# Performance work log

Hardware: AMD Instinct MI355X
Metric: run time of the kernel (lower is better)

## Reference

```python
import jax, jax.numpy as jnp
import numpy as np

B, N, DIN, DH = 16, 512, 128, 256
NEG = -9.0e15  # matches -9000000000000000.0 in torch source


def _xavier(key, fan_in, fan_out):
    lim = float(np.sqrt(6.0 / (fan_in + fan_out)))
    return jax.random.uniform(key, (fan_in, fan_out), jnp.float32, -lim, lim)


def _l2n(x, eps=1e-12):
    # torch F.normalize: x / max(||x||, eps)
    return x / jnp.maximum(jnp.linalg.norm(x, axis=-1, keepdims=True), eps)


def _prelu(x, a):
    return jnp.where(x >= 0, x, a * x)


def setup_inputs() -> dict:
    key = jax.random.key(0)
    ks = jax.random.split(key, 12)
    seq = jax.random.normal(ks[0], (B, N, DIN), jnp.float32)
    # sparse-ish nonnegative adjacency with self loops, row-normalized
    u = jax.random.uniform(ks[1], (B, N, N), jnp.float32)
    a = jnp.where(u < 0.1, u, 0.0) + jnp.eye(N, dtype=jnp.float32)[None]
    adj = a / a.sum(-1, keepdims=True)
    # dense diffusion matrix, row-normalized
    d = jax.random.uniform(ks[2], (B, N, N), jnp.float32)
    diff = d / d.sum(-1, keepdims=True)
    # dropout keep-mask for F.dropout(p=0.1, training=True)
    keep = jax.random.bernoulli(ks[3], 0.9, (B, N, N)).astype(jnp.float32)
    drop_mask = keep / 0.9
    return {
        "seq": seq, "adj": adj, "diff": diff, "drop_mask": drop_mask,
        "fc1_w": _xavier(ks[4], DIN, DH),
        "q_w": _xavier(ks[5], DH, DH),
        "k_w": _xavier(ks[6], DH, DH),
        "v_w1": _xavier(ks[7], DH, DH),
        "v_w2": _xavier(ks[8], DH, DH),
        "fc2_w": _xavier(ks[9], DIN, DH),
        "bias1": jnp.zeros((DH,), jnp.float32),
        "bias2": jnp.zeros((DH,), jnp.float32),
        "prelu1_a": jnp.float32(0.25),
        "prelu2_a": jnp.float32(0.25),
        "v_prelu_a": jnp.float32(0.25),
    }


def reference(seq, adj, diff, drop_mask, fc1_w, q_w, k_w, v_w1, v_w2,
              fc2_w, bias1, bias2, prelu1_a, prelu2_a, v_prelu_a):
    # ---- GCN1 (attention branch) ----
    fts = seq @ fc1_w                                   # [B,N,H]
    out = jnp.einsum('bmn,bnh->bmh', adj, fts)          # adj aggregation
    q = _l2n(out @ q_w)
    k = _l2n(out @ k_w)
    scores = jax.lax.stop_gradient(jnp.einsum('bmd,bnd->bmn', q, k))  # .detach()
    div_loss = jnp.mean(jnp.sum((q - k) ** 2, axis=-1))
    att = jnp.where(adj > 0, scores, NEG)
    att = jax.nn.softmax(att, axis=-1) * drop_mask      # dropout(p=0.1)
    agg = jnp.einsum('bmn,bnh->bmh', att, out)
    v = _prelu(agg @ v_w1, v_prelu_a) @ v_w2 + bias1
    h1 = _prelu(v, prelu1_a)
    # ---- GCN2 (plain branch) ----
    h2 = _prelu(jnp.einsum('bmn,bnh->bmh', diff, seq @ fc2_w) + bias2, prelu2_a)
    # ---- Readout ----
    c1 = jnp.mean(h1, axis=1)                           # [B,H]
    c2 = jnp.mean(h2, axis=1)
    # ---- DIS ----
    n1 = _l2n(h1).reshape(B * N, DH)
    n2 = _l2n(h2).reshape(B * N, DH)
    node_logits = n1 @ n2.T                             # [B*N, B*N]
    graph_logits = _l2n(c1) @ _l2n(c2).T                # [B, B]
    return node_logits, graph_logits, div_loss
```

## Files before the change

kernel.cpp:

```cpp
#include <hip/hip_runtime.h>
#include <hip/hip_bf16.h>


using bf16x8 = __attribute__((ext_vector_type(8))) short;
using f32x4  = __attribute__((ext_vector_type(4))) float;

__device__ __forceinline__ unsigned short f2b(float f) {
    union { float f; unsigned int u; } x; x.f = f;
    unsigned int r = x.u + 0x7FFFu + ((x.u >> 16) & 1u);
    return (unsigned short)(r >> 16);
}
__device__ __forceinline__ void gload_lds16(const void* g, void* l) {
    __builtin_amdgcn_global_load_lds(
        (const __attribute__((address_space(1))) void*)g,
        (__attribute__((address_space(3))) void*)l, 16, 0, 0);
}

__global__ __launch_bounds__(256) void conv3(const float* __restrict__ seq,
                                             const float* __restrict__ adj,
                                             const float* __restrict__ diff,
                                             unsigned short* __restrict__ seq_bf,
                                             unsigned short* __restrict__ adj_bf,
                                             unsigned short* __restrict__ diff_bf) {
    long i = (long)blockIdx.x * 256 + threadIdx.x;
    const float* src; unsigned short* dst; long off;
    if (i < 262144)       { src = seq;  dst = seq_bf;  off = i; }
    else if (i < 1310720) { src = adj;  dst = adj_bf;  off = i - 262144; }
    else                  { src = diff; dst = diff_bf; off = i - 1310720; }
    float4 v = reinterpret_cast<const float4*>(src)[off];
    ushort4 o; o.x = f2b(v.x); o.y = f2b(v.y); o.z = f2b(v.z); o.w = f2b(v.w);
    reinterpret_cast<ushort4*>(dst)[off] = o;
}

__global__ void wtrans6(const float* __restrict__ fc1, const float* __restrict__ fc2,
                        const float* __restrict__ qw,  const float* __restrict__ kw,
                        const float* __restrict__ v1,  const float* __restrict__ v2,
                        unsigned short* fc1T, unsigned short* fc2T,
                        unsigned short* qwT,  unsigned short* kwT,
                        unsigned short* v1T,  unsigned short* v2T) {
    __shared__ float t[32][33];
    const int z = blockIdx.z;
    const float* in; unsigned short* op; int R;
    const int C = 256;
    if      (z == 0) { in = fc1; op = fc1T; R = 128; }
    else if (z == 1) { in = fc2; op = fc2T; R = 128; }
    else if (z == 2) { in = qw;  op = qwT;  R = 256; }
    else if (z == 3) { in = kw;  op = kwT;  R = 256; }
    else if (z == 4) { in = v1;  op = v1T;  R = 256; }
    else             { in = v2;  op = v2T;  R = 256; }
    int c0 = blockIdx.x * 32, r0 = blockIdx.y * 32;
    if (r0 >= R) return;
    int x = threadIdx.x, y = threadIdx.y;
    for (int i = 0; i < 32; i += 8) t[y + i][x] = in[(long)(r0 + y + i) * C + c0 + x];
    __syncthreads();
    for (int i = 0; i < 32; i += 8)
        op[(long)(c0 + y + i) * R + r0 + x] = f2b(t[x][y + i]);
}

#define BN 128
#define BK 64

template<int TBM, int EPI, bool WF, bool WB, bool WT, bool SWZ>
__global__ __launch_bounds__(256) void gemm_nt(
    const unsigned short* __restrict__ A, const unsigned short* __restrict__ Bt,
    float* __restrict__ Cf, unsigned short* __restrict__ Cb, unsigned short* __restrict__ Ct,
    int M, int Nn, int K, int lda, int ldb, int ldc, int ldt,
    long sA, long sB, long sC, long sT,
    const float* __restrict__ bias, const float* __restrict__ alpha_ptr)
{
    constexpr int MI = TBM / 32;
    __shared__ unsigned short As[TBM][BK];
    __shared__ unsigned short Bs[BN][BK];
    const int b = blockIdx.z;
    A  += (long)b * sA;
    Bt += (long)b * sB;
    const long cbase = (long)b * sC;
    const long tbase = (long)b * sT;

    int tx, ty;
    if (SWZ) {
        int bid = blockIdx.y * gridDim.x + blockIdx.x;
        int nwg = gridDim.x * gridDim.y;
        int cpx = nwg >> 3;
        int s = (bid & 7) * cpx + (bid >> 3);
        tx = s % gridDim.x; ty = s / gridDim.x;
    } else { tx = blockIdx.x; ty = blockIdx.y; }
    const int tile_m = ty * TBM;
    const int tile_n = tx * BN;

    const int tid  = threadIdx.x;
    const int lane = tid & 63;
    const int wave = tid >> 6;
    const int wm = (wave >> 1) * (TBM / 2);
    const int wn = (wave & 1) << 6;
    const int lrow = lane >> 3;
    const int lcol = (lane & 7) << 3;

    f32x4 acc[MI][4] = {};

    for (int k0 = 0; k0 < K; k0 += BK) {
        #pragma unroll
        for (int i = 0; i < TBM / 32; ++i) {
            const int rb = (i * 4 + wave) * 8;
            gload_lds16(A + (long)(tile_m + rb + lrow) * lda + k0 + lcol, &As[rb][0]);
        }
        #pragma unroll
        for (int i = 0; i < 4; ++i) {
            const int rb = (i * 4 + wave) * 8;
            gload_lds16(Bt + (long)(tile_n + rb + lrow) * ldb + k0 + lcol, &Bs[rb][0]);
        }
        __syncthreads();
        #pragma unroll
        for (int ks = 0; ks < 2; ++ks) {
            const int kk = ks * 32 + ((lane >> 4) << 3);
            bf16x8 af[MI], bq[4];
            #pragma unroll
            for (int mi = 0; mi < MI; ++mi)
                af[mi] = *reinterpret_cast<const bf16x8*>(&As[wm + (lane & 15) + mi * 16][kk]);
            #pragma unroll
            for (int ni = 0; ni < 4; ++ni)
                bq[ni] = *reinterpret_cast<const bf16x8*>(&Bs[wn + (lane & 15) + ni * 16][kk]);
            #pragma unroll
            for (int mi = 0; mi < MI; ++mi)
                #pragma unroll
                for (int ni = 0; ni < 4; ++ni)
                    acc[mi][ni] = __builtin_amdgcn_mfma_f32_16x16x32_bf16(
                        af[mi], bq[ni], acc[mi][ni], 0, 0, 0);
        }
        __syncthreads();
    }

    const float alpha = (EPI & 1) ? alpha_ptr[0] : 0.f;
    const int c0 = lane & 15;
    const int r0 = (lane >> 4) << 2;
    #pragma unroll
    for (int ni = 0; ni < 4; ++ni) {
        const int col = tile_n + wn + ni * 16 + c0;
        const float bv = (EPI & 2) ? bias[col] : 0.f;
        #pragma unroll
        for (int mi = 0; mi < MI; ++mi) {
            const int row0 = tile_m + wm + mi * 16 + r0;
            float v[4];
            #pragma unroll
            for (int j = 0; j < 4; ++j) {
                float x = acc[mi][ni][j] + bv;
                if (EPI & 1) x = (x >= 0.f) ? x : alpha * x;
                v[j] = x;
            }
            if (WF) {
                #pragma unroll
                for (int j = 0; j < 4; ++j)
                    Cf[cbase + (long)(row0 + j) * ldc + col] = v[j];
            }
            if (WB) {
                #pragma unroll
                for (int j = 0; j < 4; ++j)
                    Cb[cbase + (long)(row0 + j) * ldc + col] = f2b(v[j]);
            }
            if (WT) {
                ushort4 o; o.x = f2b(v[0]); o.y = f2b(v[1]); o.z = f2b(v[2]); o.w = f2b(v[3]);
                *reinterpret_cast<ushort4*>(&Ct[tbase + (long)col * ldt + row0]) = o;
            }
        }
    }
}

__global__ __launch_bounds__(256) void gemm_norm(
    const unsigned short* __restrict__ A, const unsigned short* __restrict__ Bt,
    unsigned short* __restrict__ n_out, float* __restrict__ psum,
    const float* __restrict__ bias, const float* __restrict__ alpha_ptr,
    int K, int lda, int ldb, long sA, long sB)
{
    __shared__ unsigned short As[32][BK];
    __shared__ unsigned short Bs[256][BK];
    __shared__ float rowred[32][4];
    A  += (long)blockIdx.z * sA;
    Bt += (long)blockIdx.z * sB;
    const int p = blockIdx.z * gridDim.y + blockIdx.y;
    const int arow0 = blockIdx.y * 32;
    const long grow0 = (long)p * 32;

    const int tid  = threadIdx.x;
    const int lane = tid & 63;
    const int wave = tid >> 6;
    const int wn = wave << 6;
    const int lrow = lane >> 3;
    const int lcol = (lane & 7) << 3;

    f32x4 acc[2][4] = {};

    for (int k0 = 0; k0 < K; k0 += BK) {
        {
            const int rb = wave * 8;
            gload_lds16(A + (long)(arow0 + rb + lrow) * lda + k0 + lcol, &As[rb][0]);
        }
        #pragma unroll
        for (int i = 0; i < 8; ++i) {
            const int rb = (i * 4 + wave) * 8;
            gload_lds16(Bt + (long)(rb + lrow) * ldb + k0 + lcol, &Bs[rb][0]);
        }
        __syncthreads();
        #pragma unroll
        for (int ks = 0; ks < 2; ++ks) {
            const int kk = ks * 32 + ((lane >> 4) << 3);
            bf16x8 af[2], bq[4];
            #pragma unroll
            for (int mi = 0; mi < 2; ++mi)
                af[mi] = *reinterpret_cast<const bf16x8*>(&As[(lane & 15) + mi * 16][kk]);
            #pragma unroll
            for (int ni = 0; ni < 4; ++ni)
                bq[ni] = *reinterpret_cast<const bf16x8*>(&Bs[wn + (lane & 15) + ni * 16][kk]);
            #pragma unroll
            for (int mi = 0; mi < 2; ++mi)
                #pragma unroll
                for (int ni = 0; ni < 4; ++ni)
                    acc[mi][ni] = __builtin_amdgcn_mfma_f32_16x16x32_bf16(
                        af[mi], bq[ni], acc[mi][ni], 0, 0, 0);
        }
        __syncthreads();
    }

    const float alpha = alpha_ptr[0];
    const int c0 = lane & 15;
    const int r0 = (lane >> 4) << 2;
    float rs[2][4] = {};
    #pragma unroll
    for (int ni = 0; ni < 4; ++ni) {
        const float bv = bias[wn + ni * 16 + c0];
        #pragma unroll
        for (int mi = 0; mi < 2; ++mi)
            #pragma unroll
            for (int j = 0; j < 4; ++j) {
                float x = acc[mi][ni][j] + bv;
                x = (x >= 0.f) ? x : alpha * x;
                acc[mi][ni][j] = x;
                rs[mi][j] += x * x;
            }
    }
    #pragma unroll
    for (int o = 1; o <= 8; o <<= 1)
        #pragma unroll
        for (int mi = 0; mi < 2; ++mi)
            #pragma unroll
            for (int j = 0; j < 4; ++j) rs[mi][j] += __shfl_xor(rs[mi][j], o);
    if ((lane & 15) == 0) {
        #pragma unroll
        for (int mi = 0; mi < 2; ++mi)
            #pragma unroll
            for (int j = 0; j < 4; ++j) rowred[mi * 16 + r0 + j][wave] = rs[mi][j];
    }
    __syncthreads();
    float inv[2][4];
    #pragma unroll
    for (int mi = 0; mi < 2; ++mi)
        #pragma unroll
        for (int j = 0; j < 4; ++j) {
            const int r = mi * 16 + r0 + j;
            float s = rowred[r][0] + rowred[r][1] + rowred[r][2] + rowred[r][3];
            inv[mi][j] = 1.f / fmaxf(sqrtf(s), 1e-12f);
        }
    float cs[4];
    #pragma unroll
    for (int ni = 0; ni < 4; ++ni) {
        float s = 0.f;
        #pragma unroll
        for (int mi = 0; mi < 2; ++mi)
            #pragma unroll
            for (int j = 0; j < 4; ++j) s += acc[mi][ni][j];
        s += __shfl_xor(s, 16);
        s += __shfl_xor(s, 32);
        cs[ni] = s;
    }
    if (lane < 16) {
        #pragma unroll
        for (int ni = 0; ni < 4; ++ni)
            psum[(long)p * 256 + wn + ni * 16 + lane] = cs[ni];
    }
    #pragma unroll
    for (int ni = 0; ni < 4; ++ni)
        #pragma unroll
        for (int mi = 0; mi < 2; ++mi)
            #pragma unroll
            for (int j = 0; j < 4; ++j)
                n_out[(grow0 + mi * 16 + r0 + j) * 256 + wn + ni * 16 + c0] =
                    f2b(acc[mi][ni][j] * inv[mi][j]);
}

__global__ __launch_bounds__(256) void qk_proj(
    const unsigned short* __restrict__ outb,
    const unsigned short* __restrict__ qkT,
    unsigned short* __restrict__ q_bf,
    unsigned short* __restrict__ k_bf)
{
    __shared__ unsigned short As[32 * 64];
    __shared__ unsigned short Bs[512 * 64];
    __shared__ float sred[32][4];
    const long m0 = (long)blockIdx.x * 32;
    const int tid = threadIdx.x, lane = tid & 63, wave = tid >> 6;
    const int lrow = lane >> 3, lcol = (lane & 7) << 3;
    const int hi = lane >> 4, c0 = lane & 15, r0 = hi << 2;
    const int wn = wave << 7;

    f32x4 acc[2][8] = {};
    for (int k0 = 0; k0 < 256; k0 += 64) {
        gload_lds16(outb + (m0 + wave * 8 + lrow) * 256 + k0 + lcol, &As[wave * 8 * 64]);
        #pragma unroll
        for (int i = 0; i < 16; ++i) {
            const int rb = (i * 4 + wave) * 8;
            gload_lds16(qkT + (long)(rb + lrow) * 256 + k0 + lcol, &Bs[rb * 64]);
        }
        __syncthreads();
        #pragma unroll
        for (int ks = 0; ks < 2; ++ks) {
            const int kk = ks * 32 + (hi << 3);
            bf16x8 af[2], bq[8];
            #pragma unroll
            for (int mi = 0; mi < 2; ++mi)
                af[mi] = *reinterpret_cast<const bf16x8*>(&As[(mi * 16 + c0) * 64 + kk]);
            #pragma unroll
            for (int ni = 0; ni < 8; ++ni)
                bq[ni] = *reinterpret_cast<const bf16x8*>(&Bs[(wn + ni * 16 + c0) * 64 + kk]);
            #pragma unroll
            for (int mi = 0; mi < 2; ++mi)
                #pragma unroll
                for (int ni = 0; ni < 8; ++ni)
                    acc[mi][ni] = __builtin_amdgcn_mfma_f32_16x16x32_bf16(
                        af[mi], bq[ni], acc[mi][ni], 0, 0, 0);
        }
        __syncthreads();
    }
    float rs[2][4] = {};
    #pragma unroll
    for (int mi = 0; mi < 2; ++mi)
        #pragma unroll
        for (int ni = 0; ni < 8; ++ni)
            #pragma unroll
            for (int j = 0; j < 4; ++j) { float x = acc[mi][ni][j]; rs[mi][j] += x * x; }
    #pragma unroll
    for (int o = 1; o <= 8; o <<= 1)
        #pragma unroll
        for (int mi = 0; mi < 2; ++mi)
            #pragma unroll
            for (int j = 0; j < 4; ++j) rs[mi][j] += __shfl_xor(rs[mi][j], o);
    if (c0 == 0) {
        #pragma unroll
        for (int mi = 0; mi < 2; ++mi)
            #pragma unroll
            for (int j = 0; j < 4; ++j) sred[mi * 16 + r0 + j][wave] = rs[mi][j];
    }
    __syncthreads();
    float inv[2][4];
    #pragma unroll
    for (int mi = 0; mi < 2; ++mi)
        #pragma unroll
        for (int j = 0; j < 4; ++j) {
            const int r = mi * 16 + r0 + j;
            float sq = sred[r][0] + sred[r][1];
            float sk = sred[r][2] + sred[r][3];
            inv[mi][j] = 1.f / fmaxf(sqrtf(wave < 2 ? sq : sk), 1e-12f);
        }
    #pragma unroll
    for (int mi = 0; mi < 2; ++mi)
        #pragma unroll
        for (int ni = 0; ni < 8; ++ni)
            #pragma unroll
            for (int j = 0; j < 4; ++j) {
                const long rowg = m0 + mi * 16 + r0 + j;
                const int col = wn + ni * 16 + c0;
                unsigned short v = f2b(acc[mi][ni][j] * inv[mi][j]);
                if (wave < 2) q_bf[rowg * 256 + col] = v;
                else          k_bf[rowg * 256 + col - 256] = v;
            }
}

__global__ __launch_bounds__(256) void att_fused(
    const unsigned short* __restrict__ q_bf,
    const unsigned short* __restrict__ k_bf,
    const unsigned short* __restrict__ adj_bf,
    const float* __restrict__ drop,
    const unsigned short* __restrict__ outT,
    unsigned short* __restrict__ agg_bf,
    float* __restrict__ rowpart)
{
    __shared__ unsigned char smem[69632];
    unsigned short* As  = (unsigned short*)smem;
    unsigned short* Bs  = (unsigned short*)(smem + 4096);
    unsigned short* Pls = (unsigned short*)smem;
    unsigned short* Bs2 = (unsigned short*)(smem + 34816);
    __shared__ float redm[32][4], reds[32][4];

    const int b  = blockIdx.y;
    const int m0 = blockIdx.x << 5;
    const unsigned short* qp = q_bf + (long)b * 131072 + (long)m0 * 256;
    const unsigned short* kp = k_bf + (long)b * 131072;
    const unsigned short* ot = outT + (long)b * 131072;
    const unsigned short* ap = adj_bf + ((long)b * 512 + m0) * 512;
    const float*          dp = drop   + ((long)b * 512 + m0) * 512;

    const int tid = threadIdx.x, lane = tid & 63, wave = tid >> 6;
    const int lrow = lane >> 3, lcol = (lane & 7) << 3;
    const int hi = lane >> 4, c0 = lane & 15, r0 = hi << 2;
    const int wn = wave << 7;

    f32x4 acc[2][8] = {};
    for (int k0 = 0; k0 < 256; k0 += 64) {
        gload_lds16(qp + (long)(wave * 8 + lrow) * 256 + k0 + lcol, &As[wave * 8 * 64]);
        #pragma unroll
        for (int i = 0; i < 16; ++i) {
            const int rb = (i * 4 + wave) * 8;
            gload_lds16(kp + (long)(rb + lrow) * 256 + k0 + lcol, &Bs[rb * 64]);
        }
        __syncthreads();
        #pragma unroll
        for (int ks = 0; ks < 2; ++ks) {
            const int kk = ks * 32 + (hi << 3);
            bf16x8 af[2], bq[8];
            #pragma unroll
            for (int mi = 0; mi < 2; ++mi)
                af[mi] = *reinterpret_cast<const bf16x8*>(&As[(mi * 16 + c0) * 64 + kk]);
            #pragma unroll
            for (int ni = 0; ni < 8; ++ni)
                bq[ni] = *reinterpret_cast<const bf16x8*>(&Bs[(wn + ni * 16 + c0) * 64 + kk]);
            #pragma unroll
            for (int mi = 0; mi < 2; ++mi)
                #pragma unroll
                for (int ni = 0; ni < 8; ++ni)
                    acc[mi][ni] = __builtin_amdgcn_mfma_f32_16x16x32_bf16(
                        af[mi], bq[ni], acc[mi][ni], 0, 0, 0);
        }
        __syncthreads();
    }

    float rmax[2][4];
    #pragma unroll
    for (int mi = 0; mi < 2; ++mi)
        #pragma unroll
        for (int j = 0; j < 4; ++j) rmax[mi][j] = -3.0e38f;
    #pragma unroll
    for (int mi = 0; mi < 2; ++mi)
        #pragma unroll
        for (int ni = 0; ni < 8; ++ni)
            #pragma unroll
            for (int j = 0; j < 4; ++j) {
                const int rowl = mi * 16 + r0 + j;
                const int col  = wn + ni * 16 + c0;
                float s = acc[mi][ni][j];
                if (col == m0 + rowl)
                    rowpart[(long)b * 512 + m0 + rowl] = 2.f - 2.f * s;
                bool m = ap[(long)rowl * 512 + col] != 0;
                s = m ? s : -3.0e38f;
                acc[mi][ni][j] = s;
                rmax[mi][j] = fmaxf(rmax[mi][j], s);
            }
    #pragma unroll
    for (int o = 1; o <= 8; o <<= 1)
        #pragma unroll
        for (int mi = 0; mi < 2; ++mi)
            #pragma unroll
            for (int j = 0; j < 4; ++j) rmax[mi][j] = fmaxf(rmax[mi][j], __shfl_xor(rmax[mi][j], o));
    if (c0 == 0) {
        #pragma unroll
        for (int mi = 0; mi < 2; ++mi)
            #pragma unroll
            for (int j = 0; j < 4; ++j) redm[mi * 16 + r0 + j][wave] = rmax[mi][j];
    }
    __syncthreads();
    float mx[2][4], rsum[2][4];
    #pragma unroll
    for (int mi = 0; mi < 2; ++mi)
        #pragma unroll
        for (int j = 0; j < 4; ++j) {
            const int r = mi * 16 + r0 + j;
            mx[mi][j] = fmaxf(fmaxf(redm[r][0], redm[r][1]), fmaxf(redm[r][2], redm[r][3]));
            rsum[mi][j] = 0.f;
        }
    #pragma unroll
    for (int mi = 0; mi < 2; ++mi)
        #pragma unroll
        for (int ni = 0; ni < 8; ++ni)
            #pragma unroll
            for (int j = 0; j < 4; ++j) {
                float e = __expf(acc[mi][ni][j] - mx[mi][j]);
                acc[mi][ni][j] = e;
                rsum[mi][j] += e;
            }
    #pragma unroll
    for (int o = 1; o <= 8; o <<= 1)
        #pragma unroll
        for (int mi = 0; mi < 2; ++mi)
            #pragma unroll
            for (int j = 0; j < 4; ++j) rsum[mi][j] += __shfl_xor(rsum[mi][j], o);
    if (c0 == 0) {
        #pragma unroll
        for (int mi = 0; mi < 2; ++mi)
            #pragma unroll
            for (int j = 0; j < 4; ++j) reds[mi * 16 + r0 + j][wave] = rsum[mi][j];
    }
    __syncthreads();
    float inv[2][4];
    #pragma unroll
    for (int mi = 0; mi < 2; ++mi)
        #pragma unroll
        for (int j = 0; j < 4; ++j) {
            const int r = mi * 16 + r0 + j;
            inv[mi][j] = 1.f / (reds[r][0] + reds[r][1] + reds[r][2] + reds[r][3]);
        }
    #pragma unroll
    for (int mi = 0; mi < 2; ++mi)
        #pragma unroll
        for (int ni = 0; ni < 8; ++ni)
            #pragma unroll
            for (int j = 0; j < 4; ++j) {
                const int rowl = mi * 16 + r0 + j;
                const int col  = wn + ni * 16 + c0;
                float p = acc[mi][ni][j] * inv[mi][j] * dp[(long)rowl * 512 + col];
                Pls[rowl * 520 + col] = f2b(p);
            }
    __syncthreads();

    f32x4 acc2[2][4] = {};
    for (int k0 = 0; k0 < 512; k0 += 64) {
        #pragma unroll
        for (int i = 0; i < 8; ++i) {
            const int rb = (i * 4 + wave) * 8;
            gload_lds16(ot + (long)(rb + lrow) * 512 + k0 + lcol, &Bs2[rb * 64]);
        }
        __syncthreads();
        #pragma unroll
        for (int ks = 0; ks < 2; ++ks) {
            const int kk = ks * 32 + (hi << 3);
            bf16x8 af[2], bq[4];
            #pragma unroll
            for (int mi = 0; mi < 2; ++mi)
                af[mi] = *reinterpret_cast<const bf16x8*>(&Pls[(mi * 16 + c0) * 520 + k0 + kk]);
            #pragma unroll
            for (int ni = 0; ni < 4; ++ni)
                bq[ni] = *reinterpret_cast<const bf16x8*>(&Bs2[((wave << 6) + ni * 16 + c0) * 64 + kk]);
            #pragma unroll
            for (int mi = 0; mi < 2; ++mi)
                #pragma unroll
                for (int ni = 0; ni < 4; ++ni)
                    acc2[mi][ni] = __builtin_amdgcn_mfma_f32_16x16x32_bf16(
                        af[mi], bq[ni], acc2[mi][ni], 0, 0, 0);
        }
        __syncthreads();
    }
    #pragma unroll
    for (int mi = 0; mi < 2; ++mi)
        #pragma unroll
        for (int ni = 0; ni < 4; ++ni)
            #pragma unroll
            for (int j = 0; j < 4; ++j) {
                const int rowl = mi * 16 + r0 + j;
                const int col  = (wave << 6) + ni * 16 + c0;
                agg_bf[((long)b * 512 + m0 + rowl) * 256 + col] = f2b(acc2[mi][ni][j]);
            }
}

__global__ __launch_bounds__(256) void mlp_norm(
    const unsigned short* __restrict__ agg,
    const unsigned short* __restrict__ w1T,
    const unsigned short* __restrict__ w2T,
    const float* __restrict__ bias,
    const float* __restrict__ av, const float* __restrict__ a1,
    unsigned short* __restrict__ n_out,
    float* __restrict__ psum)
{
    __shared__ unsigned char smem[49664];
    unsigned short* As  = (unsigned short*)smem;
    unsigned short* Bs  = (unsigned short*)(smem + 4096);
    unsigned short* T   = (unsigned short*)smem;
    unsigned short* Bs2 = (unsigned short*)(smem + 16896);
    __shared__ float rowred[32][4];

    const int p = blockIdx.x;
    const long row0 = (long)p * 32;
    const int tid = threadIdx.x, lane = tid & 63, wave = tid >> 6;
    const int lrow = lane >> 3, lcol = (lane & 7) << 3;
    const int hi = lane >> 4, c0 = lane & 15, r0 = hi << 2;
    const int wn = wave << 6;

    f32x4 acc[2][4] = {};
    for (int k0 = 0; k0 < 256; k0 += 64) {
        gload_lds16(agg + (row0 + wave * 8 + lrow) * 256 + k0 + lcol, &As[wave * 8 * 64]);
        #pragma unroll
        for (int i = 0; i < 8; ++i) {
            const int rb = (i * 4 + wave) * 8;
            gload_lds16(w1T + (long)(rb + lrow) * 256 + k0 + lcol, &Bs[rb * 64]);
        }
        __syncthreads();
        #pragma unroll
        for (int ks = 0; ks < 2; ++ks) {
            const int kk = ks * 32 + (hi << 3);
            bf16x8 af[2], bq[4];
            #pragma unroll
            for (int mi = 0; mi < 2; ++mi)
                af[mi] = *reinterpret_cast<const bf16x8*>(&As[(mi * 16 + c0) * 64 + kk]);
            #pragma unroll
            for (int ni = 0; ni < 4; ++ni)
                bq[ni] = *reinterpret_cast<const bf16x8*>(&Bs[(wn + ni * 16 + c0) * 64 + kk]);
            #pragma unroll
            for (int mi = 0; mi < 2; ++mi)
                #pragma unroll
                for (int ni = 0; ni < 4; ++ni)
                    acc[mi][ni] = __builtin_amdgcn_mfma_f32_16x16x32_bf16(
                        af[mi], bq[ni], acc[mi][ni], 0, 0, 0);
        }
        __syncthreads();
    }
    const float alphav = av[0];
    #pragma unroll
    for (int mi = 0; mi < 2; ++mi)
        #pragma unroll
        for (int ni = 0; ni < 4; ++ni)
            #pragma unroll
            for (int j = 0; j < 4; ++j) {
                const int rowl = mi * 16 + r0 + j;
                const int col  = wn + ni * 16 + c0;
                float x = acc[mi][ni][j];
                x = (x >= 0.f) ? x : alphav * x;
                T[rowl * 264 + col] = f2b(x);
            }
    __syncthreads();

    f32x4 acc2[2][4] = {};
    for (int k0 = 0; k0 < 256; k0 += 64) {
        #pragma unroll
        for (int i = 0; i < 8; ++i) {
            const int rb = (i * 4 + wave) * 8;
            gload_lds16(w2T + (long)(rb + lrow) * 256 + k0 + lcol, &Bs2[rb * 64]);
        }
        __syncthreads();
        #pragma unroll
        for (int ks = 0; ks < 2; ++ks) {
            const int kk = ks * 32 + (hi << 3);
            bf16x8 af[2], bq[4];
            #pragma unroll
            for (int mi = 0; mi < 2; ++mi)
                af[mi] = *reinterpret_cast<const bf16x8*>(&T[(mi * 16 + c0) * 264 + k0 + kk]);
            #pragma unroll
            for (int ni = 0; ni < 4; ++ni)
                bq[ni] = *reinterpret_cast<const bf16x8*>(&Bs2[(wn + ni * 16 + c0) * 64 + kk]);
            #pragma unroll
            for (int mi = 0; mi < 2; ++mi)
                #pragma unroll
                for (int ni = 0; ni < 4; ++ni)
                    acc2[mi][ni] = __builtin_amdgcn_mfma_f32_16x16x32_bf16(
                        af[mi], bq[ni], acc2[mi][ni], 0, 0, 0);
        }
        __syncthreads();
    }
    const float alpha1 = a1[0];
    float rs[2][4] = {};
    #pragma unroll
    for (int ni = 0; ni < 4; ++ni) {
        const float bv = bias[wn + ni * 16 + c0];
        #pragma unroll
        for (int mi = 0; mi < 2; ++mi)
            #pragma unroll
            for (int j = 0; j < 4; ++j) {
                float x = acc2[mi][ni][j] + bv;
                x = (x >= 0.f) ? x : alpha1 * x;
                acc2[mi][ni][j] = x;
                rs[mi][j] += x * x;
            }
    }
    #pragma unroll
    for (int o = 1; o <= 8; o <<= 1)
        #pragma unroll
        for (int mi = 0; mi < 2; ++mi)
            #pragma unroll
            for (int j = 0; j < 4; ++j) rs[mi][j] += __shfl_xor(rs[mi][j], o);
    if (c0 == 0) {
        #pragma unroll
        for (int mi = 0; mi < 2; ++mi)
            #pragma unroll
            for (int j = 0; j < 4; ++j) rowred[mi * 16 + r0 + j][wave] = rs[mi][j];
    }
    __syncthreads();
    float inv[2][4];
    #pragma unroll
    for (int mi = 0; mi < 2; ++mi)
        #pragma unroll
        for (int j = 0; j < 4; ++j) {
            const int r = mi * 16 + r0 + j;
            float s = rowred[r][0] + rowred[r][1] + rowred[r][2] + rowred[r][3];
            inv[mi][j] = 1.f / fmaxf(sqrtf(s), 1e-12f);
        }
    float cs[4];
    #pragma unroll
    for (int ni = 0; ni < 4; ++ni) {
        float s = 0.f;
        #pragma unroll
        for (int mi = 0; mi < 2; ++mi)
            #pragma unroll
            for (int j = 0; j < 4; ++j) s += acc2[mi][ni][j];
        s += __shfl_xor(s, 16);
        s += __shfl_xor(s, 32);
        cs[ni] = s;
    }
    if (lane < 16) {
        #pragma unroll
        for (int ni = 0; ni < 4; ++ni)
            psum[(long)p * 256 + wn + ni * 16 + lane] = cs[ni];
    }
    #pragma unroll
    for (int mi = 0; mi < 2; ++mi)
        #pragma unroll
        for (int ni = 0; ni < 4; ++ni)
            #pragma unroll
            for (int j = 0; j < 4; ++j)
                n_out[(row0 + mi * 16 + r0 + j) * 256 + wn + ni * 16 + c0] =
                    f2b(acc2[mi][ni][j] * inv[mi][j]);
}

__global__ __launch_bounds__(256) void creduce(const float* __restrict__ psum1,
                                               const float* __restrict__ psum2,
                                               float* __restrict__ c1n,
                                               float* __restrict__ c2n) {
    const int which = blockIdx.x & 1, g = blockIdx.x >> 1;
    const float* ps = which ? psum2 : psum1;
    float* cn = which ? c2n : c1n;
    const int t = threadIdx.x;
    float s = 0.f;
    #pragma unroll
    for (int c = 0; c < 16; ++c) s += ps[(long)(g * 16 + c) * 256 + t];
    s *= (1.f / 512.f);
    float ss = s * s;
    #pragma unroll
    for (int o = 32; o; o >>= 1) ss += __shfl_xor(ss, o);
    __shared__ float red[4];
    if ((t & 63) == 0) red[t >> 6] = ss;
    __syncthreads();
    float tot = red[0] + red[1] + red[2] + red[3];
    cn[g * 256 + t] = s / fmaxf(sqrtf(tot), 1e-12f);
}

__global__ __launch_bounds__(256) void graphf3(const float* __restrict__ c1n,
                                               const float* __restrict__ c2n,
                                               const float* __restrict__ rowpart,
                                               float* __restrict__ out_g,
                                               float* __restrict__ out_div) {
    const int t = threadIdx.x, ii = t >> 4, jj = t & 15;
    float s = 0.f;
    for (int h = 0; h < 256; ++h) s += c1n[ii * 256 + h] * c2n[jj * 256 + h];
    out_g[ii * 16 + jj] = s;
    float ds = 0.f;
    for (int i = t; i < 8192; i += 256) ds += rowpart[i];
    #pragma unroll
    for (int o = 32; o; o >>= 1) ds += __shfl_xor(ds, o);
    __shared__ float red[4];
    if ((t & 63) == 0) red[t >> 6] = ds;
    __syncthreads();
    if (t == 0) out_div[0] = (red[0] + red[1] + red[2] + red[3]) * (1.f / 8192.f);
}

static constexpr long OFF_SEQ_BF  = 0;
static constexpr long OFF_FC1T    = 2097152;
static constexpr long OFF_QWT     = 2228224;
static constexpr long OFF_VW1T    = 2490368;
static constexpr long OFF_VW2T    = 2621440;
static constexpr long OFF_ROWPART = 2752512;
static constexpr long OFF_C1N     = 2785280;
static constexpr long OFF_C2N     = 2801664;
static constexpr long OFF_ADJ     = 3145728;
static constexpr long OFF_DIFF    = 11534336;
static constexpr long OFF_FTST    = 19922944;
static constexpr long OFF_OUTT    = 28311552;
static constexpr long OFF_OUTBF   = 32505856;
static constexpr long OFF_QBF     = 36700160;
static constexpr long OFF_KBF     = 40894464;
static constexpr long OFF_AGG     = 45088768;
static constexpr long OFF_PSUM    = 49283072;
static constexpr long OFF_N1      = 49807360;
static constexpr long OFF_N2      = 54001664;

extern "C" void kernel_launch(void* const* d_in, const int* in_sizes, int n_in,
                              void* d_out, int out_size, void* d_ws, size_t ws_size,
                              hipStream_t stream) {
    const float* seq      = (const float*)d_in[0];
    const float* adj      = (const float*)d_in[1];
    const float* diff     = (const float*)d_in[2];
    const float* drop     = (const float*)d_in[3];
    const float* fc1_w    = (const float*)d_in[4];
    const float* q_w      = (const float*)d_in[5];
    const float* k_w      = (const float*)d_in[6];
    const float* v_w1     = (const float*)d_in[7];
    const float* v_w2     = (const float*)d_in[8];
    const float* fc2_w    = (const float*)d_in[9];
    const float* bias1    = (const float*)d_in[10];
    const float* bias2    = (const float*)d_in[11];
    const float* prelu1_a = (const float*)d_in[12];
    const float* prelu2_a = (const float*)d_in[13];
    const float* v_prelu  = (const float*)d_in[14];
    float* out = (float*)d_out;

    char* ws = (char*)d_ws;
    unsigned short* seq_bf  = (unsigned short*)(ws + OFF_SEQ_BF);
    unsigned short* fc1T    = (unsigned short*)(ws + OFF_FC1T);
    unsigned short* fc2T    = (unsigned short*)(ws + OFF_FC1T + 65536);
    unsigned short* qwT     = (unsigned short*)(ws + OFF_QWT);
    unsigned short* kwT     = (unsigned short*)(ws + OFF_QWT + 131072);
    unsigned short* vw1T    = (unsigned short*)(ws + OFF_VW1T);
    unsigned short* vw2T    = (unsigned short*)(ws + OFF_VW2T);
    float*          rowpart = (float*)(ws + OFF_ROWPART);
    float*          c1n     = (float*)(ws + OFF_C1N);
    float*          c2n     = (float*)(ws + OFF_C2N);
    unsigned short* adj_bf  = (unsigned short*)(ws + OFF_ADJ);
    unsigned short* diff_bf = (unsigned short*)(ws + OFF_DIFF);
    unsigned short* ftsT    = (unsigned short*)(ws + OFF_FTST);
    unsigned short* fts2T   = (unsigned short*)(ws + OFF_FTST + 4194304);
    unsigned short* outT    = (unsigned short*)(ws + OFF_OUTT);
    unsigned short* out_bf  = (unsigned short*)(ws + OFF_OUTBF);
    unsigned short* q_bf    = (unsigned short*)(ws + OFF_QBF);
    unsigned short* k_bf    = (unsigned short*)(ws + OFF_KBF);
    unsigned short* agg_bf  = (unsigned short*)(ws + OFF_AGG);
    float*          psum1   = (float*)(ws + OFF_PSUM);
    float*          psum2   = (float*)(ws + OFF_PSUM + 262144);
    unsigned short* n1_bf   = (unsigned short*)(ws + OFF_N1);
    unsigned short* n2_bf   = (unsigned short*)(ws + OFF_N2);

    conv3<<<9216, 256, 0, stream>>>(seq, adj, diff, seq_bf, adj_bf, diff_bf);
    wtrans6<<<dim3(8, 8, 6), dim3(32, 8), 0, stream>>>(
        fc1_w, fc2_w, q_w, k_w, v_w1, v_w2, fc1T, fc2T, qwT, kwT, vw1T, vw2T);

    gemm_nt<64, 0, false, true, false, false><<<dim3(64, 4, 2), 256, 0, stream>>>(
        fc1T, seq_bf, nullptr, ftsT, nullptr,
        256, 8192, 128, 128, 128, 8192, 0, 32768, 0, 2097152, 0, nullptr, nullptr);

    gemm_nt<64, 0, false, true, true, false><<<dim3(2, 8, 16), 256, 0, stream>>>(
        adj_bf, ftsT, nullptr, out_bf, outT,
        512, 256, 512, 512, 8192, 256, 512, 262144, 512, 131072, 131072, nullptr, nullptr);

    gemm_norm<<<dim3(1, 16, 16), 256, 0, stream>>>(
        diff_bf, fts2T, n2_bf, psum2, bias2, prelu2_a, 512, 512, 8192, 262144, 512);

    qk_proj<<<256, 256, 0, stream>>>(out_bf, qwT, q_bf, k_bf);

    att_fused<<<dim3(16, 16), 256, 0, stream>>>(
        q_bf, k_bf, adj_bf, drop, outT, agg_bf, rowpart);

    mlp_norm<<<256, 256, 0, stream>>>(
        agg_bf, vw1T, vw2T, bias1, v_prelu, prelu1_a, n1_bf, psum1);

    creduce<<<32, 256, 0, stream>>>(psum1, psum2, c1n, c2n);
    graphf3<<<1, 256, 0, stream>>>(c1n, c2n, rowpart, out + 67108864, out + 67109120);

    gemm_nt<128, 0, true, false, false, true><<<dim3(64, 64, 1), 256, 0, stream>>>(
        n1_bf, n2_bf, out, nullptr, nullptr,
        8192, 8192, 256, 256, 256, 8192, 0, 0, 0, 0, 0, nullptr, nullptr);

    (void)in_sizes; (void)n_in; (void)out_size; (void)ws_size;
}
```

Before: 209.3 us.

## Fuse GCN1 aggregation with QK projection and attention with MLP kernels

Merges the fp32-to-bf16 conversion and weight-transpose kernels into one prep launch. Fuses the adj aggregation GEMM with the q/k projection and normalisation, keeping the aggregated rows in LDS instead of round-tripping out_bf. Fuses the attention kernel with the two-layer MLP and norm so the agg intermediate never goes to global memory. The large node-logit GEMM output switches to nontemporal stores. Together these cut launches and intermediate traffic, at the cost of more LDS per block and lower occupancy in the fused kernels.

New measurement: 212.5 us. About the same (+1.5%).

```diff
diff --git a/kernel.cpp b/kernel.cpp
--- a/kernel.cpp
+++ b/kernel.cpp
@@ -16,42 +16,43 @@
         (__attribute__((address_space(3))) void*)l, 16, 0, 0);
 }
 
-__global__ __launch_bounds__(256) void conv3(const float* __restrict__ seq,
-                                             const float* __restrict__ adj,
-                                             const float* __restrict__ diff,
-                                             unsigned short* __restrict__ seq_bf,
-                                             unsigned short* __restrict__ adj_bf,
-                                             unsigned short* __restrict__ diff_bf) {
-    long i = (long)blockIdx.x * 256 + threadIdx.x;
-    const float* src; unsigned short* dst; long off;
-    if (i < 262144)       { src = seq;  dst = seq_bf;  off = i; }
-    else if (i < 1310720) { src = adj;  dst = adj_bf;  off = i - 262144; }
-    else                  { src = diff; dst = diff_bf; off = i - 1310720; }
-    float4 v = reinterpret_cast<const float4*>(src)[off];
-    ushort4 o; o.x = f2b(v.x); o.y = f2b(v.y); o.z = f2b(v.z); o.w = f2b(v.w);
-    reinterpret_cast<ushort4*>(dst)[off] = o;
-}
-
-__global__ void wtrans6(const float* __restrict__ fc1, const float* __restrict__ fc2,
-                        const float* __restrict__ qw,  const float* __restrict__ kw,
-                        const float* __restrict__ v1,  const float* __restrict__ v2,
-                        unsigned short* fc1T, unsigned short* fc2T,
-                        unsigned short* qwT,  unsigned short* kwT,
-                        unsigned short* v1T,  unsigned short* v2T) {
+__global__ __launch_bounds__(256) void prep(
+    const float* __restrict__ seq, const float* __restrict__ adj,
+    const float* __restrict__ diff,
+    const float* __restrict__ fc1, const float* __restrict__ fc2,
+    const float* __restrict__ qw,  const float* __restrict__ kw,
+    const float* __restrict__ v1,  const float* __restrict__ v2,
+    unsigned short* __restrict__ seq_bf, unsigned short* __restrict__ adj_bf,
+    unsigned short* __restrict__ diff_bf,
+    unsigned short* fc1T, unsigned short* fc2T, unsigned short* qwT,
+    unsigned short* kwT,  unsigned short* v1T,  unsigned short* v2T)
+{
     __shared__ float t[32][33];
-    const int z = blockIdx.z;
+    const int bid = blockIdx.x, tid = threadIdx.x;
+    if (bid < 9216) {
+        long i = (long)bid * 256 + tid;
+        const float* src; unsigned short* dst; long off;
+        if (i < 262144)       { src = seq;  dst = seq_bf;  off = i; }
+        else if (i < 1310720) { src = adj;  dst = adj_bf;  off = i - 262144; }
+        else                  { src = diff; dst = diff_bf; off = i - 1310720; }
+        float4 v = reinterpret_cast<const float4*>(src)[off];
+        ushort4 o; o.x = f2b(v.x); o.y = f2b(v.y); o.z = f2b(v.z); o.w = f2b(v.w);
+        reinterpret_cast<ushort4*>(dst)[off] = o;
+        return;
+    }
+    const int r = bid - 9216;
+    const int z = r >> 6;
     const float* in; unsigned short* op; int R;
-    const int C = 256;
     if      (z == 0) { in = fc1; op = fc1T; R = 128; }
     else if (z == 1) { in = fc2; op = fc2T; R = 128; }
     else if (z == 2) { in = qw;  op = qwT;  R = 256; }
     else if (z == 3) { in = kw;  op = kwT;  R = 256; }
     else if (z == 4) { in = v1;  op = v1T;  R = 256; }
     else             { in = v2;  op = v2T;  R = 256; }
-    int c0 = blockIdx.x * 32, r0 = blockIdx.y * 32;
+    const int c0 = (r & 7) * 32, r0 = ((r >> 3) & 7) * 32;
     if (r0 >= R) return;
-    int x = threadIdx.x, y = threadIdx.y;
-    for (int i = 0; i < 32; i += 8) t[y + i][x] = in[(long)(r0 + y + i) * C + c0 + x];
+    const int x = tid & 31, y = tid >> 5;
+    for (int i = 0; i < 32; i += 8) t[y + i][x] = in[(long)(r0 + y + i) * 256 + c0 + x];
     __syncthreads();
     for (int i = 0; i < 32; i += 8)
         op[(long)(c0 + y + i) * R + r0 + x] = f2b(t[x][y + i]);
@@ -60,13 +61,12 @@
 #define BN 128
 #define BK 64
 
-template<int TBM, int EPI, bool WF, bool WB, bool WT, bool SWZ>
+template<int TBM, bool WF, bool WB, bool SWZ>
 __global__ __launch_bounds__(256) void gemm_nt(
     const unsigned short* __restrict__ A, const unsigned short* __restrict__ Bt,
-    float* __restrict__ Cf, unsigned short* __restrict__ Cb, unsigned short* __restrict__ Ct,
-    int M, int Nn, int K, int lda, int ldb, int ldc, int ldt,
-    long sA, long sB, long sC, long sT,
-    const float* __restrict__ bias, const float* __restrict__ alpha_ptr)
+    float* __restrict__ Cf, unsigned short* __restrict__ Cb,
+    int M, int Nn, int K, int lda, int ldb, int ldc,
+    long sA, long sB, long sC)
 {
     constexpr int MI = TBM / 32;
     __shared__ unsigned short As[TBM][BK];
@@ -75,7 +75,6 @@
     A  += (long)b * sA;
     Bt += (long)b * sB;
     const long cbase = (long)b * sC;
-    const long tbase = (long)b * sT;
 
     int tx, ty;
     if (SWZ) {
@@ -130,39 +129,500 @@
         __syncthreads();
     }
 
-    const float alpha = (EPI & 1) ? alpha_ptr[0] : 0.f;
     const int c0 = lane & 15;
     const int r0 = (lane >> 4) << 2;
     #pragma unroll
     for (int ni = 0; ni < 4; ++ni) {
         const int col = tile_n + wn + ni * 16 + c0;
-        const float bv = (EPI & 2) ? bias[col] : 0.f;
         #pragma unroll
         for (int mi = 0; mi < MI; ++mi) {
             const int row0 = tile_m + wm + mi * 16 + r0;
-            float v[4];
+            if (WF) {
+                #pragma unroll
+                for (int j = 0; j < 4; ++j)
+                    __builtin_nontemporal_store(acc[mi][ni][j],
+                        &Cf[cbase + (long)(row0 + j) * ldc + col]);
+            }
+            if (WB) {
+                #pragma unroll
+                for (int j = 0; j < 4; ++j)
+                    Cb[cbase + (long)(row0 + j) * ldc + col] = f2b(acc[mi][ni][j]);
+            }
+        }
+    }
+}
+
+__global__ __launch_bounds__(256) void gcn1qk(
+    const unsigned short* __restrict__ adj_bf,
+    const unsigned short* __restrict__ ftsT,
+    const unsigned short* __restrict__ qkT,
+    unsigned short* __restrict__ outT,
+    unsigned short* __restrict__ q_bf,
+    unsigned short* __restrict__ k_bf)
+{
+    __shared__ unsigned char smem[86528];
+    unsigned short* Ot  = (unsigned short*)smem;
+    unsigned short* As  = (unsigned short*)(smem + 16896);
+    unsigned short* Bs  = (unsigned short*)(smem + 20992);
+    unsigned short* Bs2 = (unsigned short*)(smem + 20992);
+    __shared__ float sred[32][4];
+
+    const int b  = blockIdx.y;
+    const int m0 = blockIdx.x << 5;
+    const unsigned short* ap = adj_bf + ((long)b * 512 + m0) * 512;
+
+    const int tid = threadIdx.x, lane = tid & 63, wave = tid >> 6;
+    const int lrow = lane >> 3, lcol = (lane & 7) << 3;
+    const int hi = lane >> 4, c0 = lane & 15, r0 = hi << 2;
+
+    {
+        const int wn = wave << 6;
+        f32x4 acc[2][4] = {};
+        for (int k0 = 0; k0 < 512; k0 += 64) {
+            gload_lds16(ap + (long)(wave * 8 + lrow) * 512 + k0 + lcol, &As[wave * 8 * 64]);
+            #pragma unroll
+            for (int i = 0; i < 8; ++i) {
+                const int rb = (i * 4 + wave) * 8;
+                gload_lds16(ftsT + (long)(rb + lrow) * 8192 + b * 512 + k0 + lcol, &Bs[rb * 64]);
+            }
+            __syncthreads();
+            #pragma unroll
+            for (int ks = 0; ks < 2; ++ks) {
+                const int kk = ks * 32 + (hi << 3);
+                bf16x8 af[2], bq[4];
+                #pragma unroll
+                for (int mi = 0; mi < 2; ++mi)
+                    af[mi] = *reinterpret_cast<const bf16x8*>(&As[(mi * 16 + c0) * 64 + kk]);
+                #pragma unroll
+                for (int ni = 0; ni < 4; ++ni)
+                    bq[ni] = *reinterpret_cast<const bf16x8*>(&Bs[(wn + ni * 16 + c0) * 64 + kk]);
+                #pragma unroll
+                for (int mi = 0; mi < 2; ++mi)
+                    #pragma unroll
+                    for (int ni = 0; ni < 4; ++ni)
+                        acc[mi][ni] = __builtin_amdgcn_mfma_f32_16x16x32_bf16(
+                            af[mi], bq[ni], acc[mi][ni], 0, 0, 0);
+            }
+            __syncthreads();
+        }
+        #pragma unroll
+        for (int mi = 0; mi < 2; ++mi)
+            #pragma unroll
+            for (int ni = 0; ni < 4; ++ni) {
+                const int col = wn + ni * 16 + c0;
+                ushort4 o;
+                unsigned short* e = (unsigned short*)&o;
+                #pragma unroll
+                for (int j = 0; j < 4; ++j) {
+                    unsigned short v = f2b(acc[mi][ni][j]);
+                    e[j] = v;
+                    Ot[(mi * 16 + r0 + j) * 264 + col] = v;
+                }
+                *reinterpret_cast<ushort4*>(
+                    &outT[(long)b * 131072 + (long)col * 512 + m0 + mi * 16 + r0]) = o;
+            }
+    }
+    __syncthreads();
+
+    {
+        const int wn = wave << 7;
+        f32x4 acc[2][8] = {};
+        for (int k0 = 0; k0 < 256; k0 += 64) {
+            #pragma unroll
+            for (int i = 0; i < 16; ++i) {
+                const int rb = (i * 4 + wave) * 8;
+                gload_lds16(qkT + (long)(rb + lrow) * 256 + k0 + lcol, &Bs2[rb * 64]);
+            }
+            __syncthreads();
+            #pragma unroll
+            for (int ks = 0; ks < 2; ++ks) {
+                const int kk = ks * 32 + (hi << 3);
+                bf16x8 af[2], bq[8];
+                #pragma unroll
+                for (int mi = 0; mi < 2; ++mi)
+                    af[mi] = *reinterpret_cast<const bf16x8*>(&Ot[(mi * 16 + c0) * 264 + k0 + kk]);
+                #pragma unroll
+                for (int ni = 0; ni < 8; ++ni)
+                    bq[ni] = *reinterpret_cast<const bf16x8*>(&Bs2[(wn + ni * 16 + c0) * 64 + kk]);
+                #pragma unroll
+                for (int mi = 0; mi < 2; ++mi)
+                    #pragma unroll
+                    for (int ni = 0; ni < 8; ++ni)
+                        acc[mi][ni] = __builtin_amdgcn_mfma_f32_16x16x32_bf16(
+                            af[mi], bq[ni], acc[mi][ni], 0, 0, 0);
+            }
+            __syncthreads();
+        }
+        float rs[2][4] = {};
+        #pragma unroll
+        for (int mi = 0; mi < 2; ++mi)
+            #pragma unroll
+            for (int ni = 0; ni < 8; ++ni)
+                #pragma unroll
+                for (int j = 0; j < 4; ++j) { float x = acc[mi][ni][j]; rs[mi][j] += x * x; }
+        #pragma unroll
+        for (int o = 1; o <= 8; o <<= 1)
+            #pragma unroll
+            for (int mi = 0; mi < 2; ++mi)
+                #pragma unroll
+                for (int j = 0; j < 4; ++j) rs[mi][j] += __shfl_xor(rs[mi][j], o);
+        if (c0 == 0) {
+            #pragma unroll
+            for (int mi = 0; mi < 2; ++mi)
+                #pragma unroll
+                for (int j = 0; j < 4; ++j) sred[mi * 16 + r0 + j][wave] = rs[mi][j];
+        }
+        __syncthreads();
+        float inv[2][4];
+        #pragma unroll
+        for (int mi = 0; mi < 2; ++mi)
             #pragma unroll
             for (int j = 0; j < 4; ++j) {
-                float x = acc[mi][ni][j] + bv;
-                if (EPI & 1) x = (x >= 0.f) ? x : alpha * x;
-                v[j] = x;
-            }
-            if (WF) {
+                const int rr = mi * 16 + r0 + j;
+                float sq = sred[rr][0] + sred[rr][1];
+                float sk = sred[rr][2] + sred[rr][3];
+                inv[mi][j] = 1.f / fmaxf(sqrtf(wave < 2 ? sq : sk), 1e-12f);
+            }
+        #pragma unroll
+        for (int mi = 0; mi < 2; ++mi)
+            #pragma unroll
+            for (int ni = 0; ni < 8; ++ni)
+                #pragma unroll
+                for (int j = 0; j < 4; ++j) {
+                    const long rowg = (long)b * 512 + m0 + mi * 16 + r0 + j;
+                    const int col = wn + ni * 16 + c0;
+                    unsigned short v = f2b(acc[mi][ni][j] * inv[mi][j]);
+                    if (wave < 2) q_bf[rowg * 256 + col] = v;
+                    else          k_bf[rowg * 256 + col - 256] = v;
+                }
+    }
+}
+
+__global__ __launch_bounds__(256) void attmlp(
+    const unsigned short* __restrict__ q_bf,
+    const unsigned short* __restrict__ k_bf,
+    const unsigned short* __restrict__ adj_bf,
+    const float* __restrict__ drop,
+    const unsigned short* __restrict__ outT,
+    const unsigned short* __restrict__ w1T,
+    const unsigned short* __restrict__ w2T,
+    const float* __restrict__ bias,
+    const float* __restrict__ av, const float* __restrict__ a1,
+    unsigned short* __restrict__ n_out,
+    float* __restrict__ psum,
+    float* __restrict__ rowpart)
+{
+    __shared__ unsigned char smem[69632];
+    unsigned short* As  = (unsigned short*)smem;
+    unsigned short* Bs  = (unsigned short*)(smem + 4096);
+    unsigned short* Pls = (unsigned short*)smem;
+    unsigned short* Bs2 = (unsigned short*)(smem + 34816);
+    unsigned short* T   = (unsigned short*)smem;
+    unsigned short* Bs3 = (unsigned short*)(smem + 16896);
+    __shared__ float redm[32][4], reds[32][4];
+
+    const int b  = blockIdx.y;
+    const int m0 = blockIdx.x << 5;
+    const unsigned short* qp = q_bf + (long)b * 131072 + (long)m0 * 256;
+    const unsigned short* kp = k_bf + (long)b * 131072;
+    const unsigned short* ot = outT + (long)b * 131072;
+    const unsigned short* ap = adj_bf + ((long)b * 512 + m0) * 512;
+    const float*          dp = drop   + ((long)b * 512 + m0) * 512;
+
+    const int tid = threadIdx.x, lane = tid & 63, wave = tid >> 6;
+    const int lrow = lane >> 3, lcol = (lane & 7) << 3;
+    const int hi = lane >> 4, c0 = lane & 15, r0 = hi << 2;
+
+    {
+        const int wn = wave << 7;
+        f32x4 acc[2][8] = {};
+        for (int k0 = 0; k0 < 256; k0 += 64) {
+            gload_lds16(qp + (long)(wave * 8 + lrow) * 256 + k0 + lcol, &As[wave * 8 * 64]);
+            #pragma unroll
+            for (int i = 0; i < 16; ++i) {
+                const int rb = (i * 4 + wave) * 8;
+                gload_lds16(kp + (long)(rb + lrow) * 256 + k0 + lcol, &Bs[rb * 64]);
+            }
+            __syncthreads();
+            #pragma unroll
+            for (int ks = 0; ks < 2; ++ks) {
+                const int kk = ks * 32 + (hi << 3);
+                bf16x8 af[2], bq[8];
+                #pragma unroll
+                for (int mi = 0; mi < 2; ++mi)
+                    af[mi] = *reinterpret_cast<const bf16x8*>(&As[(mi * 16 + c0) * 64 + kk]);
+                #pragma unroll
+                for (int ni = 0; ni < 8; ++ni)
+                    bq[ni] = *reinterpret_cast<const bf16x8*>(&Bs[(wn + ni * 16 + c0) * 64 + kk]);
+                #pragma unroll
+                for (int mi = 0; mi < 2; ++mi)
+                    #pragma unroll
+                    for (int ni = 0; ni < 8; ++ni)
+                        acc[mi][ni] = __builtin_amdgcn_mfma_f32_16x16x32_bf16(
+                            af[mi], bq[ni], acc[mi][ni], 0, 0, 0);
+            }
+            __syncthreads();
+        }
+
+        float rmax[2][4];
+        #pragma unroll
+        for (int mi = 0; mi < 2; ++mi)
+            #pragma unroll
+            for (int j = 0; j < 4; ++j) rmax[mi][j] = -3.0e38f;
+        #pragma unroll
+        for (int mi = 0; mi < 2; ++mi)
+            #pragma unroll
+            for (int ni = 0; ni < 8; ++ni)
+                #pragma unroll
+                for (int j = 0; j < 4; ++j) {
+                    const int rowl = mi * 16 + r0 + j;
+                    const int col  = wn + ni * 16 + c0;
+                    float s = acc[mi][ni][j];
+                    if (col == m0 + rowl)
+                        rowpart[(long)b * 512 + m0 + rowl] = 2.f - 2.f * s;
+                    bool m = ap[(long)rowl * 512 + col] != 0;
+                    s = m ? s : -3.0e38f;
+                    acc[mi][ni][j] = s;
+                    rmax[mi][j] = fmaxf(rmax[mi][j], s);
+                }
+        #pragma unroll
+        for (int o = 1; o <= 8; o <<= 1)
+            #pragma unroll
+            for (int mi = 0; mi < 2; ++mi)
                 #pragma unroll
                 for (int j = 0; j < 4; ++j)
-                    Cf[cbase + (long)(row0 + j) * ldc + col] = v[j];
-            }
-            if (WB) {
-                #pragma unroll
-                for (int j = 0; j < 4; ++j)
-                    Cb[cbase + (long)(row0 + j) * ldc + col] = f2b(v[j]);
-            }
-            if (WT) {
-                ushort4 o; o.x = f2b(v[0]); o.y = f2b(v[1]); o.z = f2b(v[2]); o.w = f2b(v[3]);
-                *reinterpret_cast<ushort4*>(&Ct[tbase + (long)col * ldt + row0]) = o;
-            }
-        }
-    }
+                    rmax[mi][j] = fmaxf(rmax[mi][j], __shfl_xor(rmax[mi][j], o));
+        if (c0 == 0) {
+            #pragma unroll
+            for (int mi = 0; mi < 2; ++mi)
+                #pragma unroll
+                for (int j = 0; j < 4; ++j) redm[mi * 16 + r0 + j][wave] = rmax[mi][j];
+        }
+        __syncthreads();
+        float mx[2][4], rsum[2][4];
+        #pragma unroll
+        for (int mi = 0; mi < 2; ++mi)
+            #pragma unroll
+            for (int j = 0; j < 4; ++j) {
+                const int rr = mi * 16 + r0 + j;
+                mx[mi][j] = fmaxf(fmaxf(redm[rr][0], redm[rr][1]), fmaxf(redm[rr][2], redm[rr][3]));
+                rsum[mi][j] = 0.f;
+            }
+        #pragma unroll
+        for (int mi = 0; mi < 2; ++mi)
+            #pragma unroll
+            for (int ni = 0; ni < 8; ++ni)
+                #pragma unroll
+                for (int j = 0; j < 4; ++j) {
+                    float e = __expf(acc[mi][ni][j] - mx[mi][j]);
+                    acc[mi][ni][j] = e;
+                    rsum[mi][j] += e;
+                }
+        #pragma unroll
+        for (int o = 1; o <= 8; o <<= 1)
+            #pragma unroll
+            for (int mi = 0; mi < 2; ++mi)
+                #pragma unroll
+                for (int j = 0; j < 4; ++j) rsum[mi][j] += __shfl_xor(rsum[mi][j], o);
+        if (c0 == 0) {
+            #pragma unroll
+            for (int mi = 0; mi < 2; ++mi)
+                #pragma unroll
+                for (int j = 0; j < 4; ++j) reds[mi * 16 + r0 + j][wave] = rsum[mi][j];
+        }
+        __syncthreads();
+        float inv[2][4];
+        #pragma unroll
+        for (int mi = 0; mi < 2; ++mi)
+            #pragma unroll
+            for (int j = 0; j < 4; ++j) {
+                const int rr = mi * 16 + r0 + j;
+                inv[mi][j] = 1.f / (reds[rr][0] + reds[rr][1] + reds[rr][2] + reds[rr][3]);
+            }
+        #pragma unroll
+        for (int mi = 0; mi < 2; ++mi)
+            #pragma unroll
+            for (int ni = 0; ni < 8; ++ni)
+                #pragma unroll
+                for (int j = 0; j < 4; ++j) {
+                    const int rowl = mi * 16 + r0 + j;
+                    const int col  = wn + ni * 16 + c0;
+                    float p = acc[mi][ni][j] * inv[mi][j] * dp[(long)rowl * 512 + col];
+                    Pls[rowl * 520 + col] = f2b(p);
+                }
+    }
+    __syncthreads();
+
+    f32x4 acc2[2][4] = {};
+    {
+        const int wn = wave << 6;
+        for (int k0 = 0; k0 < 512; k0 += 64) {
+            #pragma unroll
+            for (int i = 0; i < 8; ++i) {
+                const int rb = (i * 4 + wave) * 8;
+                gload_lds16(ot + (long)(rb + lrow) * 512 + k0 + lcol, &Bs2[rb * 64]);
+            }
+            __syncthreads();
+            #pragma unroll
+            for (int ks = 0; ks < 2; ++ks) {
+                const int kk = ks * 32 + (hi << 3);
+                bf16x8 af[2], bq[4];
+                #pragma unroll
+                for (int mi = 0; mi < 2; ++mi)
+                    af[mi] = *reinterpret_cast<const bf16x8*>(&Pls[(mi * 16 + c0) * 520 + k0 + kk]);
+                #pragma unroll
+                for (int ni = 0; ni < 4; ++ni)
+                    bq[ni] = *reinterpret_cast<const bf16x8*>(&Bs2[(wn + ni * 16 + c0) * 64 + kk]);
+                #pragma unroll
+                for (int mi = 0; mi < 2; ++mi)
+                    #pragma unroll
+                    for (int ni = 0; ni < 4; ++ni)
+                        acc2[mi][ni] = __builtin_amdgcn_mfma_f32_16x16x32_bf16(
+                            af[mi], bq[ni], acc2[mi][ni], 0, 0, 0);
+            }
+            __syncthreads();
+        }
+    }
+
+    const int wn6 = wave << 6;
+    const float alphav = av[0];
+    #pragma unroll
+    for (int mi = 0; mi < 2; ++mi)
+        #pragma unroll
+        for (int ni = 0; ni < 4; ++ni)
+            #pragma unroll
+            for (int j = 0; j < 4; ++j)
+                T[(mi * 16 + r0 + j) * 264 + wn6 + ni * 16 + c0] = f2b(acc2[mi][ni][j]);
+    f32x4 acct[2][4] = {};
+    for (int k0 = 0; k0 < 256; k0 += 64) {
+        #pragma unroll
+        for (int i = 0; i < 8; ++i) {
+            const int rb = (i * 4 + wave) * 8;
+            gload_lds16(w1T + (long)(rb + lrow) * 256 + k0 + lcol, &Bs3[rb * 64]);
+        }
+        __syncthreads();
+        #pragma unroll
+        for (int ks = 0; ks < 2; ++ks) {
+            const int kk = ks * 32 + (hi << 3);
+            bf16x8 af[2], bq[4];
+            #pragma unroll
+            for (int mi = 0; mi < 2; ++mi)
+                af[mi] = *reinterpret_cast<const bf16x8*>(&T[(mi * 16 + c0) * 264 + k0 + kk]);
+            #pragma unroll
+            for (int ni = 0; ni < 4; ++ni)
+                bq[ni] = *reinterpret_cast<const bf16x8*>(&Bs3[(wn6 + ni * 16 + c0) * 64 + kk]);
+            #pragma unroll
+            for (int mi = 0; mi < 2; ++mi)
+                #pragma unroll
+                for (int ni = 0; ni < 4; ++ni)
+                    acct[mi][ni] = __builtin_amdgcn_mfma_f32_16x16x32_bf16(
+                        af[mi], bq[ni], acct[mi][ni], 0, 0, 0);
+        }
+        __syncthreads();
+    }
+    #pragma unroll
+    for (int mi = 0; mi < 2; ++mi)
+        #pragma unroll
+        for (int ni = 0; ni < 4; ++ni)
+            #pragma unroll
+            for (int j = 0; j < 4; ++j) {
+                float x = acct[mi][ni][j];
+                x = (x >= 0.f) ? x : alphav * x;
+                T[(mi * 16 + r0 + j) * 264 + wn6 + ni * 16 + c0] = f2b(x);
+            }
+
+    f32x4 acc3[2][4] = {};
+    for (int k0 = 0; k0 < 256; k0 += 64) {
+        #pragma unroll
+        for (int i = 0; i < 8; ++i) {
+            const int rb = (i * 4 + wave) * 8;
+            gload_lds16(w2T + (long)(rb + lrow) * 256 + k0 + lcol, &Bs3[rb * 64]);
+        }
+        __syncthreads();
+        #pragma unroll
+        for (int ks = 0; ks < 2; ++ks) {
+            const int kk = ks * 32 + (hi << 3);
+            bf16x8 af[2], bq[4];
+            #pragma unroll
+            for (int mi = 0; mi < 2; ++mi)
+                af[mi] = *reinterpret_cast<const bf16x8*>(&T[(mi * 16 + c0) * 264 + k0 + kk]);
+            #pragma unroll
+            for (int ni = 0; ni < 4; ++ni)
+                bq[ni] = *reinterpret_cast<const bf16x8*>(&Bs3[(wn6 + ni * 16 + c0) * 64 + kk]);
+            #pragma unroll
+            for (int mi = 0; mi < 2; ++mi)
+                #pragma unroll
+                for (int ni = 0; ni < 4; ++ni)
+                    acc3[mi][ni] = __builtin_amdgcn_mfma_f32_16x16x32_bf16(
+                        af[mi], bq[ni], acc3[mi][ni], 0, 0, 0);
+        }
+        __syncthreads();
+    }
+
+    const float alpha1 = a1[0];
+    float rs[2][4] = {};
+    #pragma unroll
+    for (int ni = 0; ni < 4; ++ni) {
+        const float bv = bias[wn6 + ni * 16 + c0];
+        #pragma unroll
+        for (int mi = 0; mi < 2; ++mi)
+            #pragma unroll
+            for (int j = 0; j < 4; ++j) {
+                float x = acc3[mi][ni][j] + bv;
+                x = (x >= 0.f) ? x : alpha1 * x;
+                acc3[mi][ni][j] = x;
+                rs[mi][j] += x * x;
+            }
+    }
+    #pragma unroll
+    for (int o = 1; o <= 8; o <<= 1)
+        #pragma unroll
+        for (int mi = 0; mi < 2; ++mi)
+            #pragma unroll
+            for (int j = 0; j < 4; ++j) rs[mi][j] += __shfl_xor(rs[mi][j], o);
+    if (c0 == 0) {
+        #pragma unroll
+        for (int mi = 0; mi < 2; ++mi)
+            #pragma unroll
+            for (int j = 0; j < 4; ++j) redm[mi * 16 + r0 + j][wave] = rs[mi][j];
+    }
+    __syncthreads();
+    float inv2[2][4];
+    #pragma unroll
+    for (int mi = 0; mi < 2; ++mi)
+        #pragma unroll
+        for (int j = 0; j < 4; ++j) {
+            const int rr = mi * 16 + r0 + j;
+            float s = redm[rr][0] + redm[rr][1] + redm[rr][2] + redm[rr][3];
+            inv2[mi][j] = 1.f / fmaxf(sqrtf(s), 1e-12f);
+        }
+    float cs[4];
+    #pragma unroll
+    for (int ni = 0; ni < 4; ++ni) {
+        float s = 0.f;
+        #pragma unroll
+        for (int mi = 0; mi < 2; ++mi)
+            #pragma unroll
+            for (int j = 0; j < 4; ++j) s += acc3[mi][ni][j];
+        s += __shfl_xor(s, 16);
+        s += __shfl_xor(s, 32);
+        cs[ni] = s;
+    }
+    const int p = b * 16 + blockIdx.x;
+    if (lane < 16) {
+        #pragma unroll
+        for (int ni = 0; ni < 4; ++ni)
+            psum[(long)p * 256 + wn6 + ni * 16 + lane] = cs[ni];
+    }
+    const long row0g = (long)b * 512 + m0;
+    #pragma unroll
+    for (int mi = 0; mi < 2; ++mi)
+        #pragma unroll
+        for (int ni = 0; ni < 4; ++ni)
+            #pragma unroll
+            for (int j = 0; j < 4; ++j)
+                n_out[(row0g + mi * 16 + r0 + j) * 256 + wn6 + ni * 16 + c0] =
+                    f2b(acc3[mi][ni][j] * inv2[mi][j]);
 }
 
 __global__ __launch_bounds__(256) void gemm_norm(
@@ -286,434 +746,6 @@
                     f2b(acc[mi][ni][j] * inv[mi][j]);
 }
 
-__global__ __launch_bounds__(256) void qk_proj(
-    const unsigned short* __restrict__ outb,
-    const unsigned short* __restrict__ qkT,
-    unsigned short* __restrict__ q_bf,
-    unsigned short* __restrict__ k_bf)
-{
-    __shared__ unsigned short As[32 * 64];
-    __shared__ unsigned short Bs[512 * 64];
-    __shared__ float sred[32][4];
-    const long m0 = (long)blockIdx.x * 32;
-    const int tid = threadIdx.x, lane = tid & 63, wave = tid >> 6;
-    const int lrow = lane >> 3, lcol = (lane & 7) << 3;
-    const int hi = lane >> 4, c0 = lane & 15, r0 = hi << 2;
-    const int wn = wave << 7;
-
-    f32x4 acc[2][8] = {};
-    for (int k0 = 0; k0 < 256; k0 += 64) {
-        gload_lds16(outb + (m0 + wave * 8 + lrow) * 256 + k0 + lcol, &As[wave * 8 * 64]);
-        #pragma unroll
-        for (int i = 0; i < 16; ++i) {
-            const int rb = (i * 4 + wave) * 8;
-            gload_lds16(qkT + (long)(rb + lrow) * 256 + k0 + lcol, &Bs[rb * 64]);
-        }
-        __syncthreads();
-        #pragma unroll
-        for (int ks = 0; ks < 2; ++ks) {
-            const int kk = ks * 32 + (hi << 3);
-            bf16x8 af[2], bq[8];
-            #pragma unroll
-            for (int mi = 0; mi < 2; ++mi)
-                af[mi] = *reinterpret_cast<const bf16x8*>(&As[(mi * 16 + c0) * 64 + kk]);
-            #pragma unroll
-            for (int ni = 0; ni < 8; ++ni)
-                bq[ni] = *reinterpret_cast<const bf16x8*>(&Bs[(wn + ni * 16 + c0) * 64 + kk]);
-            #pragma unroll
-            for (int mi = 0; mi < 2; ++mi)
-                #pragma unroll
-                for (int ni = 0; ni < 8; ++ni)
-                    acc[mi][ni] = __builtin_amdgcn_mfma_f32_16x16x32_bf16(
-                        af[mi], bq[ni], acc[mi][ni], 0, 0, 0);
-        }
-        __syncthreads();
-    }
-    float rs[2][4] = {};
-    #pragma unroll
-    for (int mi = 0; mi < 2; ++mi)
-        #pragma unroll
-        for (int ni = 0; ni < 8; ++ni)
-            #pragma unroll
-            for (int j = 0; j < 4; ++j) { float x = acc[mi][ni][j]; rs[mi][j] += x * x; }
-    #pragma unroll
-    for (int o = 1; o <= 8; o <<= 1)
-        #pragma unroll
-        for (int mi = 0; mi < 2; ++mi)
-            #pragma unroll
-            for (int j = 0; j < 4; ++j) rs[mi][j] += __shfl_xor(rs[mi][j], o);
-    if (c0 == 0) {
-        #pragma unroll
-        for (int mi = 0; mi < 2; ++mi)
-            #pragma unroll
-            for (int j = 0; j < 4; ++j) sred[mi * 16 + r0 + j][wave] = rs[mi][j];
-    }
-    __syncthreads();
-    float inv[2][4];
-    #pragma unroll
-    for (int mi = 0; mi < 2; ++mi)
-        #pragma unroll
-        for (int j = 0; j < 4; ++j) {
-            const int r = mi * 16 + r0 + j;
-            float sq = sred[r][0] + sred[r][1];
-            float sk = sred[r][2] + sred[r][3];
-            inv[mi][j] = 1.f / fmaxf(sqrtf(wave < 2 ? sq : sk), 1e-12f);
-        }
-    #pragma unroll
-    for (int mi = 0; mi < 2; ++mi)
-        #pragma unroll
-        for (int ni = 0; ni < 8; ++ni)
-            #pragma unroll
-            for (int j = 0; j < 4; ++j) {
-                const long rowg = m0 + mi * 16 + r0 + j;
-                const int col = wn + ni * 16 + c0;
-                unsigned short v = f2b(acc[mi][ni][j] * inv[mi][j]);
-                if (wave < 2) q_bf[rowg * 256 + col] = v;
-                else          k_bf[rowg * 256 + col - 256] = v;
-            }
-}
-
-__global__ __launch_bounds__(256) void att_fused(
-    const unsigned short* __restrict__ q_bf,
-    const unsigned short* __restrict__ k_bf,
-    const unsigned short* __restrict__ adj_bf,
-    const float* __restrict__ drop,
-    const unsigned short* __restrict__ outT,
-    unsigned short* __restrict__ agg_bf,
-    float* __restrict__ rowpart)
-{
-    __shared__ unsigned char smem[69632];
-    unsigned short* As  = (unsigned short*)smem;
-    unsigned short* Bs  = (unsigned short*)(smem + 4096);
-    unsigned short* Pls = (unsigned short*)smem;
-    unsigned short* Bs2 = (unsigned short*)(smem + 34816);
-    __shared__ float redm[32][4], reds[32][4];
-
-    const int b  = blockIdx.y;
-    const int m0 = blockIdx.x << 5;
-    const unsigned short* qp = q_bf + (long)b * 131072 + (long)m0 * 256;
-    const unsigned short* kp = k_bf + (long)b * 131072;
-    const unsigned short* ot = outT + (long)b * 131072;
-    const unsigned short* ap = adj_bf + ((long)b * 512 + m0) * 512;
-    const float*          dp = drop   + ((long)b * 512 + m0) * 512;
-
-    const int tid = threadIdx.x, lane = tid & 63, wave = tid >> 6;
-    const int lrow = lane >> 3, lcol = (lane & 7) << 3;
-    const int hi = lane >> 4, c0 = lane & 15, r0 = hi << 2;
-    const int wn = wave << 7;
-
-    f32x4 acc[2][8] = {};
-    for (int k0 = 0; k0 < 256; k0 += 64) {
-        gload_lds16(qp + (long)(wave * 8 + lrow) * 256 + k0 + lcol, &As[wave * 8 * 64]);
-        #pragma unroll
-        for (int i = 0; i < 16; ++i) {
-            const int rb = (i * 4 + wave) * 8;
-            gload_lds16(kp + (long)(rb + lrow) * 256 + k0 + lcol, &Bs[rb * 64]);
-        }
-        __syncthreads();
-        #pragma unroll
-        for (int ks = 0; ks < 2; ++ks) {
-            const int kk = ks * 32 + (hi << 3);
-            bf16x8 af[2], bq[8];
-            #pragma unroll
-            for (int mi = 0; mi < 2; ++mi)
-                af[mi] = *reinterpret_cast<const bf16x8*>(&As[(mi * 16 + c0) * 64 + kk]);
-            #pragma unroll
-            for (int ni = 0; ni < 8; ++ni)
-                bq[ni] = *reinterpret_cast<const bf16x8*>(&Bs[(wn + ni * 16 + c0) * 64 + kk]);
-            #pragma unroll
-            for (int mi = 0; mi < 2; ++mi)
-                #pragma unroll
-                for (int ni = 0; ni < 8; ++ni)
-                    acc[mi][ni] = __builtin_amdgcn_mfma_f32_16x16x32_bf16(
-                        af[mi], bq[ni], acc[mi][ni], 0, 0, 0);
-        }
-        __syncthreads();
-    }
-
-    float rmax[2][4];
-    #pragma unroll
-    for (int mi = 0; mi < 2; ++mi)
-        #pragma unroll
-        for (int j = 0; j < 4; ++j) rmax[mi][j] = -3.0e38f;
-    #pragma unroll
-    for (int mi = 0; mi < 2; ++mi)
-        #pragma unroll
-        for (int ni = 0; ni < 8; ++ni)
-            #pragma unroll
-            for (int j = 0; j < 4; ++j) {
-                const int rowl = mi * 16 + r0 + j;
-                const int col  = wn + ni * 16 + c0;
-                float s = acc[mi][ni][j];
-                if (col == m0 + rowl)
-                    rowpart[(long)b * 512 + m0 + rowl] = 2.f - 2.f * s;
-                bool m = ap[(long)rowl * 512 + col] != 0;
-                s = m ? s : -3.0e38f;
-                acc[mi][ni][j] = s;
-                rmax[mi][j] = fmaxf(rmax[mi][j], s);
-            }
-    #pragma unroll
-    for (int o = 1; o <= 8; o <<= 1)
-        #pragma unroll
-        for (int mi = 0; mi < 2; ++mi)
-            #pragma unroll
-            for (int j = 0; j < 4; ++j) rmax[mi][j] = fmaxf(rmax[mi][j], __shfl_xor(rmax[mi][j], o));
-    if (c0 == 0) {
-        #pragma unroll
-        for (int mi = 0; mi < 2; ++mi)
-            #pragma unroll
-            for (int j = 0; j < 4; ++j) redm[mi * 16 + r0 + j][wave] = rmax[mi][j];
-    }
-    __syncthreads();
-    float mx[2][4], rsum[2][4];
-    #pragma unroll
-    for (int mi = 0; mi < 2; ++mi)
-        #pragma unroll
-        for (int j = 0; j < 4; ++j) {
-            const int r = mi * 16 + r0 + j;
-            mx[mi][j] = fmaxf(fmaxf(redm[r][0], redm[r][1]), fmaxf(redm[r][2], redm[r][3]));
-            rsum[mi][j] = 0.f;
-        }
-    #pragma unroll
-    for (int mi = 0; mi < 2; ++mi)
-        #pragma unroll
-        for (int ni = 0; ni < 8; ++ni)
-            #pragma unroll
-            for (int j = 0; j < 4; ++j) {
-                float e = __expf(acc[mi][ni][j] - mx[mi][j]);
-                acc[mi][ni][j] = e;
-                rsum[mi][j] += e;
-            }
-    #pragma unroll
-    for (int o = 1; o <= 8; o <<= 1)
-        #pragma unroll
-        for (int mi = 0; mi < 2; ++mi)
-            #pragma unroll
-            for (int j = 0; j < 4; ++j) rsum[mi][j] += __shfl_xor(rsum[mi][j], o);
-    if (c0 == 0) {
-        #pragma unroll
-        for (int mi = 0; mi < 2; ++mi)
-            #pragma unroll
-            for (int j = 0; j < 4; ++j) reds[mi * 16 + r0 + j][wave] = rsum[mi][j];
-    }
-    __syncthreads();
-    float inv[2][4];
-    #pragma unroll
-    for (int mi = 0; mi < 2; ++mi)
-        #pragma unroll
-        for (int j = 0; j < 4; ++j) {
-            const int r = mi * 16 + r0 + j;
-            inv[mi][j] = 1.f / (reds[r][0] + reds[r][1] + reds[r][2] + reds[r][3]);
-        }
-    #pragma unroll
-    for (int mi = 0; mi < 2; ++mi)
-        #pragma unroll
-        for (int ni = 0; ni < 8; ++ni)
-            #pragma unroll
-            for (int j = 0; j < 4; ++j) {
-                const int rowl = mi * 16 + r0 + j;
-                const int col  = wn + ni * 16 + c0;
-                float p = acc[mi][ni][j] * inv[mi][j] * dp[(long)rowl * 512 + col];
-                Pls[rowl * 520 + col] = f2b(p);
-            }
-    __syncthreads();
-
-    f32x4 acc2[2][4] = {};
-    for (int k0 = 0; k0 < 512; k0 += 64) {
-        #pragma unroll
-        for (int i = 0; i < 8; ++i) {
-            const int rb = (i * 4 + wave) * 8;
-            gload_lds16(ot + (long)(rb + lrow) * 512 + k0 + lcol, &Bs2[rb * 64]);
-        }
-        __syncthreads();
-        #pragma unroll
-        for (int ks = 0; ks < 2; ++ks) {
-            const int kk = ks * 32 + (hi << 3);
-            bf16x8 af[2], bq[4];
-            #pragma unroll
-            for (int mi = 0; mi < 2; ++mi)
-                af[mi] = *reinterpret_cast<const bf16x8*>(&Pls[(mi * 16 + c0) * 520 + k0 + kk]);
-            #pragma unroll
-            for (int ni = 0; ni < 4; ++ni)
-                bq[ni] = *reinterpret_cast<const bf16x8*>(&Bs2[((wave << 6) + ni * 16 + c0) * 64 + kk]);
-            #pragma unroll
-            for (int mi = 0; mi < 2; ++mi)
-                #pragma unroll
-                for (int ni = 0; ni < 4; ++ni)
-                    acc2[mi][ni] = __builtin_amdgcn_mfma_f32_16x16x32_bf16(
-                        af[mi], bq[ni], acc2[mi][ni], 0, 0, 0);
-        }
-        __syncthreads();
-    }
-    #pragma unroll
-    for (int mi = 0; mi < 2; ++mi)
-        #pragma unroll
-        for (int ni = 0; ni < 4; ++ni)
-            #pragma unroll
-            for (int j = 0; j < 4; ++j) {
-                const int rowl = mi * 16 + r0 + j;
-                const int col  = (wave << 6) + ni * 16 + c0;
-                agg_bf[((long)b * 512 + m0 + rowl) * 256 + col] = f2b(acc2[mi][ni][j]);
-            }
-}
-
-__global__ __launch_bounds__(256) void mlp_norm(
-    const unsigned short* __restrict__ agg,
-    const unsigned short* __restrict__ w1T,
-    const unsigned short* __restrict__ w2T,
-    const float* __restrict__ bias,
-    const float* __restrict__ av, const float* __restrict__ a1,
-    unsigned short* __restrict__ n_out,
-    float* __restrict__ psum)
-{
-    __shared__ unsigned char smem[49664];
-    unsigned short* As  = (unsigned short*)smem;
-    unsigned short* Bs  = (unsigned short*)(smem + 4096);
-    unsigned short* T   = (unsigned short*)smem;
-    unsigned short* Bs2 = (unsigned short*)(smem + 16896);
-    __shared__ float rowred[32][4];
-
-    const int p = blockIdx.x;
-    const long row0 = (long)p * 32;
-    const int tid = threadIdx.x, lane = tid & 63, wave = tid >> 6;
-    const int lrow = lane >> 3, lcol = (lane & 7) << 3;
-    const int hi = lane >> 4, c0 = lane & 15, r0 = hi << 2;
-    const int wn = wave << 6;
-
-    f32x4 acc[2][4] = {};
-    for (int k0 = 0; k0 < 256; k0 += 64) {
-        gload_lds16(agg + (row0 + wave * 8 + lrow) * 256 + k0 + lcol, &As[wave * 8 * 64]);
-        #pragma unroll
-        for (int i = 0; i < 8; ++i) {
-            const int rb = (i * 4 + wave) * 8;
-            gload_lds16(w1T + (long)(rb + lrow) * 256 + k0 + lcol, &Bs[rb * 64]);
-        }
-        __syncthreads();
-        #pragma unroll
-        for (int ks = 0; ks < 2; ++ks) {
-            const int kk = ks * 32 + (hi << 3);
-            bf16x8 af[2], bq[4];
-            #pragma unroll
-            for (int mi = 0; mi < 2; ++mi)
-                af[mi] = *reinterpret_cast<const bf16x8*>(&As[(mi * 16 + c0) * 64 + kk]);
-            #pragma unroll
-            for (int ni = 0; ni < 4; ++ni)
-                bq[ni] = *reinterpret_cast<const bf16x8*>(&Bs[(wn + ni * 16 + c0) * 64 + kk]);
-            #pragma unroll
-            for (int mi = 0; mi < 2; ++mi)
-                #pragma unroll
-                for (int ni = 0; ni < 4; ++ni)
-                    acc[mi][ni] = __builtin_amdgcn_mfma_f32_16x16x32_bf16(
-                        af[mi], bq[ni], acc[mi][ni], 0, 0, 0);
-        }
-        __syncthreads();
-    }
-    const float alphav = av[0];
-    #pragma unroll
-    for (int mi = 0; mi < 2; ++mi)
-        #pragma unroll
-        for (int ni = 0; ni < 4; ++ni)
-            #pragma unroll
-            for (int j = 0; j < 4; ++j) {
-                const int rowl = mi * 16 + r0 + j;
-                const int col  = wn + ni * 16 + c0;
-                float x = acc[mi][ni][j];
-                x = (x >= 0.f) ? x : alphav * x;
-                T[rowl * 264 + col] = f2b(x);
-            }
-    __syncthreads();
-
-    f32x4 acc2[2][4] = {};
-    for (int k0 = 0; k0 < 256; k0 += 64) {
-        #pragma unroll
-        for (int i = 0; i < 8; ++i) {
-            const int rb = (i * 4 + wave) * 8;
-            gload_lds16(w2T + (long)(rb + lrow) * 256 + k0 + lcol, &Bs2[rb * 64]);
-        }
-        __syncthreads();
-        #pragma unroll
-        for (int ks = 0; ks < 2; ++ks) {
-            const int kk = ks * 32 + (hi << 3);
-            bf16x8 af[2], bq[4];
-            #pragma unroll
-            for (int mi = 0; mi < 2; ++mi)
-                af[mi] = *reinterpret_cast<const bf16x8*>(&T[(mi * 16 + c0) * 264 + k0 + kk]);
-            #pragma unroll
-            for (int ni = 0; ni < 4; ++ni)
-                bq[ni] = *reinterpret_cast<const bf16x8*>(&Bs2[(wn + ni * 16 + c0) * 64 + kk]);
-            #pragma unroll
-            for (int mi = 0; mi < 2; ++mi)
-                #pragma unroll
-                for (int ni = 0; ni < 4; ++ni)
-                    acc2[mi][ni] = __builtin_amdgcn_mfma_f32_16x16x32_bf16(
-                        af[mi], bq[ni], acc2[mi][ni], 0, 0, 0);
-        }
-        __syncthreads();
-    }
-    const float alpha1 = a1[0];
-    float rs[2][4] = {};
-    #pragma unroll
-    for (int ni = 0; ni < 4; ++ni) {
-        const float bv = bias[wn + ni * 16 + c0];
-        #pragma unroll
-        for (int mi = 0; mi < 2; ++mi)
-            #pragma unroll
-            for (int j = 0; j < 4; ++j) {
-                float x = acc2[mi][ni][j] + bv;
-                x = (x >= 0.f) ? x : alpha1 * x;
-                acc2[mi][ni][j] = x;
-                rs[mi][j] += x * x;
-            }
-    }
-    #pragma unroll
-    for (int o = 1; o <= 8; o <<= 1)
-        #pragma unroll
-        for (int mi = 0; mi < 2; ++mi)
-            #pragma unroll
-            for (int j = 0; j < 4; ++j) rs[mi][j] += __shfl_xor(rs[mi][j], o);
-    if (c0 == 0) {
-        #pragma unroll
-        for (int mi = 0; mi < 2; ++mi)
-            #pragma unroll
-            for (int j = 0; j < 4; ++j) rowred[mi * 16 + r0 + j][wave] = rs[mi][j];
-    }
-    __syncthreads();
-    float inv[2][4];
-    #pragma unroll
-    for (int mi = 0; mi < 2; ++mi)
-        #pragma unroll
-        for (int j = 0; j < 4; ++j) {
-            const int r = mi * 16 + r0 + j;
-            float s = rowred[r][0] + rowred[r][1] + rowred[r][2] + rowred[r][3];
-            inv[mi][j] = 1.f / fmaxf(sqrtf(s), 1e-12f);
-        }
-    float cs[4];
-    #pragma unroll
-    for (int ni = 0; ni < 4; ++ni) {
-        float s = 0.f;
-        #pragma unroll
-        for (int mi = 0; mi < 2; ++mi)
-            #pragma unroll
-            for (int j = 0; j < 4; ++j) s += acc2[mi][ni][j];
-        s += __shfl_xor(s, 16);
-        s += __shfl_xor(s, 32);
-        cs[ni] = s;
-    }
-    if (lane < 16) {
-        #pragma unroll
-        for (int ni = 0; ni < 4; ++ni)
-            psum[(long)p * 256 + wn + ni * 16 + lane] = cs[ni];
-    }
-    #pragma unroll
-    for (int mi = 0; mi < 2; ++mi)
-        #pragma unroll
-        for (int ni = 0; ni < 4; ++ni)
-            #pragma unroll
-            for (int j = 0; j < 4; ++j)
-                n_out[(row0 + mi * 16 + r0 + j) * 256 + wn + ni * 16 + c0] =
-                    f2b(acc2[mi][ni][j] * inv[mi][j]);
-}
-
 __global__ __launch_bounds__(256) void creduce(const float* __restrict__ psum1,
                                                const float* __restrict__ psum2,
                                                float* __restrict__ c1n,
@@ -760,20 +792,18 @@
 static constexpr long OFF_QWT     = 2228224;
 static constexpr long OFF_VW1T    = 2490368;
 static constexpr long OFF_VW2T    = 2621440;
-static constexpr long OFF_ROWPART = 2752512;
-static constexpr long OFF_C1N     = 2785280;
-static constexpr long OFF_C2N     = 2801664;
 static constexpr long OFF_ADJ     = 3145728;
 static constexpr long OFF_DIFF    = 11534336;
 static constexpr long OFF_FTST    = 19922944;
 static constexpr long OFF_OUTT    = 28311552;
-static constexpr long OFF_OUTBF   = 32505856;
-static constexpr long OFF_QBF     = 36700160;
-static constexpr long OFF_KBF     = 40894464;
-static constexpr long OFF_AGG     = 45088768;
+static constexpr long OFF_QBF     = 32505856;
+static constexpr long OFF_KBF     = 36700160;
+static constexpr long OFF_N1      = 40894464;
+static constexpr long OFF_N2      = 45088768;
 static constexpr long OFF_PSUM    = 49283072;
-static constexpr long OFF_N1      = 49807360;
-static constexpr long OFF_N2      = 54001664;
+static constexpr long OFF_ROWPART = 49807360;
+static constexpr long OFF_C1N     = 49840128;
+static constexpr long OFF_C2N     = 49856512;
 
 extern "C" void kernel_launch(void* const* d_in, const int* in_sizes, int n_in,
                               void* d_out, int out_size, void* d_ws, size_t ws_size,
@@ -803,52 +833,43 @@
     unsigned short* kwT     = (unsigned short*)(ws + OFF_QWT + 131072);
     unsigned short* vw1T    = (unsigned short*)(ws + OFF_VW1T);
     unsigned short* vw2T    = (unsigned short*)(ws + OFF_VW2T);
-    float*          rowpart = (float*)(ws + OFF_ROWPART);
-    float*          c1n     = (float*)(ws + OFF_C1N);
-    float*          c2n     = (float*)(ws + OFF_C2N);
     unsigned short* adj_bf  = (unsigned short*)(ws + OFF_ADJ);
     unsigned short* diff_bf = (unsigned short*)(ws + OFF_DIFF);
     unsigned short* ftsT    = (unsigned short*)(ws + OFF_FTST);
     unsigned short* fts2T   = (unsigned short*)(ws + OFF_FTST + 4194304);
     unsigned short* outT    = (unsigned short*)(ws + OFF_OUTT);
-    unsigned short* out_bf  = (unsigned short*)(ws + OFF_OUTBF);
     unsigned short* q_bf    = (unsigned short*)(ws + OFF_QBF);
     unsigned short* k_bf    = (unsigned short*)(ws + OFF_KBF);
-    unsigned short* agg_bf  = (unsigned short*)(ws + OFF_AGG);
+    unsigned short* n1_bf   = (unsigned short*)(ws + OFF_N1);
+    unsigned short* n2_bf   = (unsigned short*)(ws + OFF_N2);
     float*          psum1   = (float*)(ws + OFF_PSUM);
     float*          psum2   = (float*)(ws + OFF_PSUM + 262144);
-    unsigned short* n1_bf   = (unsigned short*)(ws + OFF_N1);
-    unsigned short* n2_bf   = (unsigned short*)(ws + OFF_N2);
-
-    conv3<<<9216, 256, 0, stream>>>(seq, adj, diff, seq_bf, adj_bf, diff_bf);
-    wtrans6<<<dim3(8, 8, 6), dim3(32, 8), 0, stream>>>(
-        fc1_w, fc2_w, q_w, k_w, v_w1, v_w2, fc1T, fc2T, qwT, kwT, vw1T, vw2T);
-
-    gemm_nt<64, 0, false, true, false, false><<<dim3(64, 4, 2), 256, 0, stream>>>(
-        fc1T, seq_bf, nullptr, ftsT, nullptr,
-        256, 8192, 128, 128, 128, 8192, 0, 32768, 0, 2097152, 0, nullptr, nullptr);
-
-    gemm_nt<64, 0, false, true, true, false><<<dim3(2, 8, 16), 256, 0, stream>>>(
-        adj_bf, ftsT, nullptr, out_bf, outT,
-        512, 256, 512, 512, 8192, 256, 512, 262144, 512, 131072, 131072, nullptr, nullptr);
+    float*          rowpart = (float*)(ws + OFF_ROWPART);
+    float*          c1n     = (float*)(ws + OFF_C1N);
+    float*          c2n     = (float*)(ws + OFF_C2N);
+
+    prep<<<9600, 256, 0, stream>>>(seq, adj, diff, fc1_w, fc2_w, q_w, k_w, v_w1, v_w2,
+                                   seq_bf, adj_bf, diff_bf, fc1T, fc2T, qwT, kwT, vw1T, vw2T);
+
+    gemm_nt<64, false, true, false><<<dim3(64, 4, 2), 256, 0, stream>>>(
+        fc1T, seq_bf, nullptr, ftsT,
+        256, 8192, 128, 128, 128, 8192, 32768, 0, 2097152);
+
+    gcn1qk<<<dim3(16, 16), 256, 0, stream>>>(adj_bf, ftsT, qwT, outT, q_bf, k_bf);
 
     gemm_norm<<<dim3(1, 16, 16), 256, 0, stream>>>(
         diff_bf, fts2T, n2_bf, psum2, bias2, prelu2_a, 512, 512, 8192, 262144, 512);
 
-    qk_proj<<<256, 256, 0, stream>>>(out_bf, qwT, q_bf, k_bf);
-
-    att_fused<<<dim3(16, 16), 256, 0, stream>>>(
-        q_bf, k_bf, adj_bf, drop, outT, agg_bf, rowpart);
-
-    mlp_norm<<<256, 256, 0, stream>>>(
-        agg_bf, vw1T, vw2T, bias1, v_prelu, prelu1_a, n1_bf, psum1);
+    attmlp<<<dim3(16, 16), 256, 0, stream>>>(
+        q_bf, k_bf, adj_bf, drop, outT, vw1T, vw2T, bias1, v_prelu, prelu1_a,
+        n1_bf, psum1, rowpart);
 
     creduce<<<32, 256, 0, stream>>>(psum1, psum2, c1n, c2n);
     graphf3<<<1, 256, 0, stream>>>(c1n, c2n, rowpart, out + 67108864, out + 67109120);
 
-    gemm_nt<128, 0, true, false, false, true><<<dim3(64, 64, 1), 256, 0, stream>>>(
-        n1_bf, n2_bf, out, nullptr, nullptr,
-        8192, 8192, 256, 256, 256, 8192, 0, 0, 0, 0, 0, nullptr, nullptr);
+    gemm_nt<128, true, false, true><<<dim3(64, 64, 1), 256, 0, stream>>>(
+        n1_bf, n2_bf, out, nullptr,
+        8192, 8192, 256, 256, 256, 8192, 0, 0, 0);
 
     (void)in_sizes; (void)n_in; (void)out_size; (void)ws_size;
 }
```
